# Optimization experiments

Measured on AMD Instinct MI355X. Metric: run time of the kernel, lower is better.

Reference implementation:

```python
import jax, jax.numpy as jnp
import numpy as np
import math

H = 5       # attention heads
DK = 20     # attdim // H
ATT = 100   # attdim
LAYERS = 2
B, L, BERT_DIM = 32, 256, 768


def _layernorm(x, a, b, eps=1e-6):
    mean = x.mean(-1, keepdims=True)
    std = jnp.std(x, axis=-1, ddof=1, keepdims=True)  # torch.std is unbiased
    return a * (x - mean) / (std + eps) + b


def _forward(sequence_output, src_mask, aspect_mask, short_mask,
             ln_a, ln_b, Wxx_w, Wxx_b, q_w, q_b, k_w, k_b,
             dense_w, dense_b, bias_m, W_w, W_b, Wx_w, Wx_b, clf_w, clf_b):
    Bn, Ln, _ = sequence_output.shape
    x = _layernorm(sequence_output, ln_a, ln_b)
    g = x @ Wxx_w + Wxx_b                                  # [B,L,100]
    asp_wn = aspect_mask.sum(1, keepdims=True)             # [B,1]
    aspect = (g * aspect_mask[..., None]).sum(1) / asp_wn  # [B,100]

    q = (g @ q_w + q_b).reshape(Bn, Ln, H, DK).transpose(0, 2, 1, 3)  # [B,H,L,dk]
    k = (g @ k_w + k_b).reshape(Bn, Ln, H, DK).transpose(0, 2, 1, 3)
    # aspect is expanded identically across heads/positions before dense -> [B,dk]
    asp = aspect @ dense_w + dense_b                       # [B,dk]
    scores = jnp.einsum('bhid,bhjd->bhij', q, k) / math.sqrt(DK)
    asp_sc = jnp.tanh(jnp.einsum('bd,bhjd->bhj', asp, k) + bias_m[0])
    scores = scores + asp_sc[:, :, None, :]
    scores = jnp.where(src_mask[:, None, None, :] == 0, -1e9, scores)
    scores = scores + short_mask                           # [B,1,L,L] broadcast
    adj = jax.nn.softmax(scores, axis=-1)                  # [B,H,L,L]

    # edge-update linear split so the [B,L,L,205] concat is never materialized:
    # edge[b,i,j] = adj_perm[b,i,j] @ Wa + go[b,j] @ W1 + go[b,i] @ W2 + b
    Wa, W1, W2 = Wx_w[:H], Wx_w[H:H + ATT], Wx_w[H + ATT:]
    go = g
    for i in range(LAYERS):
        # expand+matmul+mean over heads == mean-head message passing
        Ax = jnp.einsum('bhij,bjd->bid', adj, go) / H
        go = jax.nn.relu(Ax @ W_w + W_b)
        if i < LAYERS - 1:  # last edge update is discarded by the original output
            edge = (jnp.einsum('bhij,hk->bijk', adj, Wa)
                    + (go @ W1)[:, None, :, :]
                    + (go @ W2)[:, :, None, :]
                    + Wx_b)
            adj = edge.transpose(0, 3, 1, 2)
    # original: node_outputs = F.relu(gcn_outputs) (aggregate_W result is overwritten)
    h = jax.nn.relu(go)
    out1 = (h * aspect_mask[..., None]).sum(1) / asp_wn    # [B,100]
    return out1 @ clf_w + clf_b                            # [B,3]


def setup_inputs() -> dict:
    key = jax.random.key(0)
    ks = jax.random.split(key, 24)
    f32 = jnp.float32
    p = lambda k, shape, s=0.05: jax.random.normal(k, shape, dtype=f32) * s
    src_mask = jax.random.randint(ks[0], (B, L), 0, 2, dtype=jnp.int32).at[:, 0].set(1)
    aspect_mask = jnp.zeros((B, L), f32).at[:, 4:8].set(1.0)  # aspect span tokens
    return {
        'sequence_output': jax.random.normal(ks[1], (B, L, BERT_DIM), dtype=f32),
        'src_mask': src_mask,
        'aspect_mask': aspect_mask,
        'short_mask': p(ks[2], (B, 1, L, L), 1.0),
        'ln_a': jnp.ones((BERT_DIM,), f32),
        'ln_b': jnp.zeros((BERT_DIM,), f32),
        'Wxx_w': p(ks[3], (BERT_DIM, ATT)), 'Wxx_b': p(ks[4], (ATT,)),
        'q_w': p(ks[5], (ATT, ATT)), 'q_b': p(ks[6], (ATT,)),
        'k_w': p(ks[7], (ATT, ATT)), 'k_b': p(ks[8], (ATT,)),
        'dense_w': p(ks[9], (ATT, DK)), 'dense_b': p(ks[10], (DK,)),
        'bias_m': p(ks[11], (1,)),
        'W_w': p(ks[12], (ATT, ATT)), 'W_b': p(ks[13], (ATT,)),
        'Wx_w': p(ks[14], (H + 2 * ATT, H)), 'Wx_b': p(ks[15], (H,)),
        'clf_w': p(ks[16], (ATT, 3)), 'clf_b': p(ks[17], (3,)),
    }


def reference(sequence_output, src_mask, aspect_mask, short_mask,
              ln_a, ln_b, Wxx_w, Wxx_b, q_w, q_b, k_w, k_b,
              dense_w, dense_b, bias_m, W_w, W_b, Wx_w, Wx_b, clf_w, clf_b):
    return _forward(sequence_output, src_mask, aspect_mask, short_mask,
                    ln_a, ln_b, Wxx_w, Wxx_b, q_w, q_b, k_w, k_b,
                    dense_w, dense_b, bias_m, W_w, W_b, Wx_w, Wx_b, clf_w, clf_b)
```

## Files before the change

### kernel.cpp

```cpp
#include <hip/hip_runtime.h>
#include <math.h>

constexpr int CL = 256;
constexpr int CD = 768;
constexpr int CATT = 100;
constexpr int CH = 5;
constexpr int CDK = 20;

__device__ __forceinline__ void fma4(float4& a, float s, const float4& w) {
    a.x = fmaf(s, w.x, a.x);
    a.y = fmaf(s, w.y, a.y);
    a.z = fmaf(s, w.z, a.z);
    a.w = fmaf(s, w.w, a.w);
}

__global__ __launch_bounds__(256, 3) void k1_fused(
    const float* __restrict__ x, const float* __restrict__ ln_a,
    const float* __restrict__ ln_b, const float* __restrict__ Wxx_w,
    const float* __restrict__ Wxx_b, const float* __restrict__ q_w,
    const float* __restrict__ q_b, const float* __restrict__ k_w,
    const float* __restrict__ k_b, const float* __restrict__ amask,
    float* __restrict__ g, float* __restrict__ qt, float* __restrict__ ktb,
    float* __restrict__ aspect_raw)
{
    __shared__ float s_w[2][3200];
    __shared__ float s_xn[2][16 * 36];
    __shared__ float s_gt[16 * 100];
    __shared__ float s_ln[1536];
    __shared__ float s_mean[16], s_rinv[16];

    const int t = threadIdx.x;
    const int r0 = blockIdx.x * 16;
    const int wid = t >> 6, lane = t & 63;

    if (t < 192) {
        ((float4*)s_ln)[t] = ((const float4*)ln_a)[t];
        ((float4*)(s_ln + 768))[t] = ((const float4*)ln_b)[t];
    }

    for (int rr = wid * 4; rr < wid * 4 + 4; ++rr) {
        const float* xr = x + (size_t)(r0 + rr) * CD;
        float xv[12];
        float s = 0.f;
#pragma unroll
        for (int m = 0; m < 12; ++m) { xv[m] = xr[lane + 64 * m]; s += xv[m]; }
#pragma unroll
        for (int o = 32; o; o >>= 1) s += __shfl_xor(s, o);
        float mean = s * (1.0f / 768.0f);
        float sq = 0.f;
#pragma unroll
        for (int m = 0; m < 12; ++m) { float d = xv[m] - mean; sq = fmaf(d, d, sq); }
#pragma unroll
        for (int o = 32; o; o >>= 1) sq += __shfl_xor(sq, o);
        if (lane == 0) {
            s_mean[rr] = mean;
            s_rinv[rr] = 1.0f / (sqrtf(sq * (1.0f / 767.0f)) + 1e-6f);
        }
    }

    const float4* wsrc = (const float4*)Wxx_w;
    float4 w0 = wsrc[t], w1 = wsrc[t + 256], w2 = wsrc[t + 512], w3;
    if (t < 32) w3 = wsrc[t + 768];
    const int rA = t >> 5, cA = t & 31;
    float xa = x[(size_t)(r0 + rA) * CD + cA];
    float xb = x[(size_t)(r0 + rA + 8) * CD + cA];

    __syncthreads();

    {
        float4* d4 = (float4*)s_w[0];
        d4[t] = w0; d4[t + 256] = w1; d4[t + 512] = w2;
        if (t < 32) d4[t + 768] = w3;
        float la = s_ln[cA], lbv = s_ln[768 + cA];
        s_xn[0][rA * 36 + cA] = fmaf(la, (xa - s_mean[rA]) * s_rinv[rA], lbv);
        s_xn[0][(rA + 8) * 36 + cA] = fmaf(la, (xb - s_mean[rA + 8]) * s_rinv[rA + 8], lbv);
    }
    __syncthreads();

    const int cg = t % 25, rg = t / 25;
    const int c = cg * 4;
    float4 acc0 = make_float4(0.f, 0.f, 0.f, 0.f);
    float4 acc1 = make_float4(0.f, 0.f, 0.f, 0.f);

    for (int kt = 0; kt < 24; ++kt) {
        if (kt < 23) {
            const float4* ws = wsrc + (size_t)(kt + 1) * 800;
            w0 = ws[t]; w1 = ws[t + 256]; w2 = ws[t + 512];
            if (t < 32) w3 = ws[t + 768];
            int gc = (kt + 1) * 32 + cA;
            xa = x[(size_t)(r0 + rA) * CD + gc];
            xb = x[(size_t)(r0 + rA + 8) * CD + gc];
        }
        if (t < 200) {
            const float* wb = s_w[kt & 1];
            const float* xbuf = s_xn[kt & 1];
#pragma unroll 2
            for (int kk = 0; kk < 32; kk += 4) {
                float4 a0 = *(const float4*)&xbuf[(rg * 2 + 0) * 36 + kk];
                float4 a1 = *(const float4*)&xbuf[(rg * 2 + 1) * 36 + kk];
                float4 v0 = *(const float4*)&wb[(kk + 0) * 100 + c];
                float4 v1 = *(const float4*)&wb[(kk + 1) * 100 + c];
                float4 v2 = *(const float4*)&wb[(kk + 2) * 100 + c];
                float4 v3 = *(const float4*)&wb[(kk + 3) * 100 + c];
                fma4(acc0, a0.x, v0); fma4(acc0, a0.y, v1); fma4(acc0, a0.z, v2); fma4(acc0, a0.w, v3);
                fma4(acc1, a1.x, v0); fma4(acc1, a1.y, v1); fma4(acc1, a1.z, v2); fma4(acc1, a1.w, v3);
            }
        }
        if (kt < 23) {
            float4* d4 = (float4*)s_w[(kt + 1) & 1];
            d4[t] = w0; d4[t + 256] = w1; d4[t + 512] = w2;
            if (t < 32) d4[t + 768] = w3;
            int gc = (kt + 1) * 32 + cA;
            float la = s_ln[gc], lbv = s_ln[768 + gc];
            float* xd = s_xn[(kt + 1) & 1];
            xd[rA * 36 + cA] = fmaf(la, (xa - s_mean[rA]) * s_rinv[rA], lbv);
            xd[(rA + 8) * 36 + cA] = fmaf(la, (xb - s_mean[rA + 8]) * s_rinv[rA + 8], lbv);
        }
        __syncthreads();
    }

    if (t < 200) {
        float4 bias = *(const float4*)&Wxx_b[c];
        float4 rv0, rv1;
        rv0.x = acc0.x + bias.x; rv0.y = acc0.y + bias.y; rv0.z = acc0.z + bias.z; rv0.w = acc0.w + bias.w;
        rv1.x = acc1.x + bias.x; rv1.y = acc1.y + bias.y; rv1.z = acc1.z + bias.z; rv1.w = acc1.w + bias.w;
        float4 rv[2] = { rv0, rv1 };
#pragma unroll
        for (int q = 0; q < 2; ++q) {
            int row = r0 + rg * 2 + q;
            *(float4*)&g[(size_t)row * CATT + c] = rv[q];
            *(float4*)&s_gt[(rg * 2 + q) * 100 + c] = rv[q];
            float m = amask[row];
            if (m != 0.f) {
                int b = row >> 8;
                atomicAdd(&aspect_raw[b * CATT + c + 0], m * rv[q].x);
                atomicAdd(&aspect_raw[b * CATT + c + 1], m * rv[q].y);
                atomicAdd(&aspect_raw[b * CATT + c + 2], m * rv[q].z);
                atomicAdd(&aspect_raw[b * CATT + c + 3], m * rv[q].w);
            }
        }
    }

    const float4* qw4 = (const float4*)q_w;
    const float4* kw4 = (const float4*)k_w;
    float4 sA = qw4[t], sB;
    if (t < 244) sB = qw4[t + 256];
    __syncthreads();
    {
        float4* d4 = (float4*)s_w[0];
        d4[t] = sA; if (t < 244) d4[t + 256] = sB;
    }
    __syncthreads();

    float4 p0 = make_float4(0.f, 0.f, 0.f, 0.f);
    float4 p1 = make_float4(0.f, 0.f, 0.f, 0.f);
    for (int tau = 0; tau < 10; ++tau) {
        if (tau < 9) {
            const float4* src = (tau + 1 < 5) ? qw4 + (size_t)(tau + 1) * 500
                                              : kw4 + (size_t)(tau - 4) * 500;
            sA = src[t]; if (t < 244) sB = src[t + 256];
        }
        if (t < 200) {
            const float* wb = s_w[tau & 1];
            const int kb = (tau % 5) * 20;
#pragma unroll 2
            for (int kk = 0; kk < 20; kk += 4) {
                float4 a0 = *(const float4*)&s_gt[(rg * 2 + 0) * 100 + kb + kk];
                float4 a1 = *(const float4*)&s_gt[(rg * 2 + 1) * 100 + kb + kk];
                float4 v0 = *(const float4*)&wb[(kk + 0) * 100 + c];
                float4 v1 = *(const float4*)&wb[(kk + 1) * 100 + c];
                float4 v2 = *(const float4*)&wb[(kk + 2) * 100 + c];
                float4 v3 = *(const float4*)&wb[(kk + 3) * 100 + c];
                fma4(p0, a0.x, v0); fma4(p0, a0.y, v1); fma4(p0, a0.z, v2); fma4(p0, a0.w, v3);
                fma4(p1, a1.x, v0); fma4(p1, a1.y, v1); fma4(p1, a1.z, v2); fma4(p1, a1.w, v3);
            }
            if (tau == 4 || tau == 9) {
                const float* bb = (tau == 4) ? q_b : k_b;
                float* outp = (tau == 4) ? qt : ktb;
                float4 bias = *(const float4*)&bb[c];
                p0.x += bias.x; p0.y += bias.y; p0.z += bias.z; p0.w += bias.w;
                p1.x += bias.x; p1.y += bias.y; p1.z += bias.z; p1.w += bias.w;
                const int h = c / CDK, d = c % CDK;
                float4 rv[2] = { p0, p1 };
#pragma unroll
                for (int q = 0; q < 2; ++q) {
                    int row = r0 + rg * 2 + q;
                    int bidx = row >> 8, l = row & 255;
                    *(float4*)&outp[((size_t)(bidx * CH + h) * CL + l) * CDK + d] = rv[q];
                }
                p0 = make_float4(0.f, 0.f, 0.f, 0.f);
                p1 = make_float4(0.f, 0.f, 0.f, 0.f);
            }
        }
        if (tau < 9) {
            float4* d4 = (float4*)s_w[(tau + 1) & 1];
            d4[t] = sA; if (t < 244) d4[t + 256] = sB;
        }
        __syncthreads();
    }
}

__global__ __launch_bounds__(256, 3) void k45_attn_gcn0(
    const float* __restrict__ qt, const float* __restrict__ ktb,
    const float* __restrict__ aspect_raw, const float* __restrict__ amask,
    const float* __restrict__ dense_w, const float* __restrict__ dense_b,
    const float* __restrict__ bias_m, const int* __restrict__ src_mask,
    const float* __restrict__ shortm, const float* __restrict__ Wx_w,
    const float* __restrict__ g, const float* __restrict__ W_w,
    const float* __restrict__ W_b, float* __restrict__ adjW,
    float* __restrict__ go1, float* __restrict__ t1, float* __restrict__ t2,
    float* __restrict__ gW2S)
{
    constexpr int ICH = 16;
    __shared__ float s_pool[16 * 260];
    __shared__ float s_w[2][3200];
    __shared__ float s_q[CH * 320];
    __shared__ float s_red[CH][64];
    __shared__ float s_was[5];
    __shared__ float s_aspb[20];
    __shared__ float s_w1[100], s_w2[100];
    __shared__ float s_g1row[16];

    const int b = blockIdx.x >> 4, ic = blockIdx.x & 15;
    const int i0 = ic * ICH;
    const int t = threadIdx.x, lane = t & 63, wid = t >> 6;
    const int j = t;

    if (t < 5) {
        float s = 0.f;
        for (int k2 = 0; k2 < 5; ++k2) s += Wx_w[t * 5 + k2];
        s_was[t] = s;
    }
    if (t < 100) {
        float a = 0.f, c2 = 0.f;
#pragma unroll
        for (int h = 0; h < 5; ++h) {
            a += Wx_w[(5 + t) * 5 + h];
            c2 += Wx_w[(105 + t) * 5 + h];
        }
        s_w1[t] = a; s_w2[t] = c2;
    }
    float wn = 0.f;
    if (t < 64) {
        float4 mv = ((const float4*)amask)[b * 64 + t];
        wn = mv.x + mv.y + mv.z + mv.w;
#pragma unroll
        for (int o = 32; o; o >>= 1) wn += __shfl_xor(wn, o);
    }
    if (t < 20) {
        float a = 0.f;
        for (int d = 0; d < CATT; ++d)
            a = fmaf(aspect_raw[b * CATT + d], dense_w[d * CDK + t], a);
        s_aspb[t] = a / wn + dense_b[t];
    }
    {
        const float* qbase = qt + (size_t)b * CH * CL * CDK + (size_t)i0 * CDK;
        for (int i = t; i < CH * 320; i += 256) {
            int h = i / 320, r = i % 320;
            s_q[i] = qbase[(size_t)h * CL * CDK + r];
        }
    }

    const bool masked = (src_mask[b * CL + j] == 0);
    const float bm = bias_m[0];
    const float rs20 = 0.223606797749978969f;

    float sm[ICH];
#pragma unroll
    for (int ii = 0; ii < ICH; ++ii)
        sm[ii] = shortm[(size_t)(b * CL + i0 + ii) * CL + j];

    float accS[ICH], accW[ICH];
#pragma unroll
    for (int ii = 0; ii < ICH; ++ii) { accS[ii] = 0.f; accW[ii] = 0.f; }

    __syncthreads();

    for (int h = 0; h < CH; ++h) {
        float4 kr[5];
        const float* kp = ktb + ((size_t)(b * CH + h) * CL + j) * CDK;
#pragma unroll
        for (int m = 0; m < 5; ++m) kr[m] = *(const float4*)(kp + 4 * m);
        const float was_h = s_was[h];
        float s = bm;
#pragma unroll
        for (int m = 0; m < 5; ++m) {
            s = fmaf(s_aspb[4 * m + 0], kr[m].x, s);
            s = fmaf(s_aspb[4 * m + 1], kr[m].y, s);
            s = fmaf(s_aspb[4 * m + 2], kr[m].z, s);
            s = fmaf(s_aspb[4 * m + 3], kr[m].w, s);
        }
        const float aspsc = tanhf(s);

        float pv[ICH];
#pragma unroll
        for (int ii = 0; ii < ICH; ++ii) {
            const float* qrow = &s_q[h * 320 + ii * CDK];
            float sc = 0.f;
#pragma unroll
            for (int m = 0; m < 5; ++m) {
                float4 q4 = *(const float4*)(qrow + 4 * m);
                sc = fmaf(q4.x, kr[m].x, sc);
                sc = fmaf(q4.y, kr[m].y, sc);
                sc = fmaf(q4.z, kr[m].z, sc);
                sc = fmaf(q4.w, kr[m].w, sc);
            }
            sc = fmaf(sc, rs20, aspsc) + sm[ii];
            float p = masked ? 0.f : __expf(sc);
            pv[ii] = p;
            float ssum = p;
#pragma unroll
            for (int o = 32; o; o >>= 1) ssum += __shfl_xor(ssum, o);
            if (lane == 0) s_red[h][ii * 4 + wid] = ssum;
        }
        __syncthreads();
#pragma unroll
        for (int ii = 0; ii < ICH; ++ii) {
            float tot = s_red[h][ii * 4 + 0] + s_red[h][ii * 4 + 1] +
                        s_red[h][ii * 4 + 2] + s_red[h][ii * 4 + 3];
            float pn = pv[ii] * __frcp_rn(tot);
            accS[ii] += pn;
            accW[ii] = fmaf(was_h, pn, accW[ii]);
        }
    }

#pragma unroll
    for (int ii = 0; ii < ICH; ++ii) {
        adjW[(size_t)(b * CL + i0 + ii) * CL + j] = accW[ii];
        s_pool[ii * 260 + j] = accS[ii];
    }

    const int cg = t % 25, rg = t / 25;
    const int c = cg * 4;
    const float4* g4 = (const float4*)g + (size_t)b * 6400;
    float4 sA = g4[t], sB = g4[t + 256], sC = g4[t + 512], sD;
    if (t < 32) sD = g4[t + 768];
    {
        float4* d4 = (float4*)s_w[0];
        d4[t] = sA; d4[t + 256] = sB; d4[t + 512] = sC;
        if (t < 32) d4[t + 768] = sD;
    }
    __syncthreads();

    float4 acc0 = make_float4(0.f, 0.f, 0.f, 0.f);
    float4 acc1 = make_float4(0.f, 0.f, 0.f, 0.f);
    for (int jt = 0; jt < 8; ++jt) {
        if (jt < 7) {
            const float4* src = g4 + (size_t)(jt + 1) * 800;
            sA = src[t]; sB = src[t + 256]; sC = src[t + 512];
            if (t < 32) sD = src[t + 768];
        }
        if (t < 200) {
            const float* wb = s_w[jt & 1];
#pragma unroll 2
            for (int kk = 0; kk < 32; kk += 4) {
                float4 a0 = *(const float4*)&s_pool[(rg * 2 + 0) * 260 + jt * 32 + kk];
                float4 a1 = *(const float4*)&s_pool[(rg * 2 + 1) * 260 + jt * 32 + kk];
                float4 v0 = *(const float4*)&wb[(kk + 0) * 100 + c];
                float4 v1 = *(const float4*)&wb[(kk + 1) * 100 + c];
                float4 v2 = *(const float4*)&wb[(kk + 2) * 100 + c];
                float4 v3 = *(const float4*)&wb[(kk + 3) * 100 + c];
                fma4(acc0, a0.x, v0); fma4(acc0, a0.y, v1); fma4(acc0, a0.z, v2); fma4(acc0, a0.w, v3);
                fma4(acc1, a1.x, v0); fma4(acc1, a1.y, v1); fma4(acc1, a1.z, v2); fma4(acc1, a1.w, v3);
            }
        }
        if (jt < 7) {
            float4* d4 = (float4*)s_w[(jt + 1) & 1];
            d4[t] = sA; d4[t + 256] = sB; d4[t + 512] = sC;
            if (t < 32) d4[t + 768] = sD;
        }
        __syncthreads();
    }

    float* s_ax = s_pool;
    if (t < 200) {
        float4 r;
        r.x = acc0.x * 0.2f; r.y = acc0.y * 0.2f; r.z = acc0.z * 0.2f; r.w = acc0.w * 0.2f;
        *(float4*)&s_ax[(rg * 2 + 0) * 108 + c] = r;
        r.x = acc1.x * 0.2f; r.y = acc1.y * 0.2f; r.z = acc1.z * 0.2f; r.w = acc1.w * 0.2f;
        *(float4*)&s_ax[(rg * 2 + 1) * 108 + c] = r;
    }
    const float4* ww4 = (const float4*)W_w;
    sA = ww4[t]; if (t < 244) sB = ww4[t + 256];
    {
        float4* d4 = (float4*)s_w[0];
        d4[t] = sA; if (t < 244) d4[t + 256] = sB;
    }
    __syncthreads();

    float4 o0 = make_float4(0.f, 0.f, 0.f, 0.f);
    float4 o1 = make_float4(0.f, 0.f, 0.f, 0.f);
    for (int wt = 0; wt < 5; ++wt) {
        if (wt < 4) {
            const float4* src = ww4 + (size_t)(wt + 1) * 500;
            sA = src[t]; if (t < 244) sB = src[t + 256];
        }
        if (t < 200) {
            const float* wb = s_w[wt & 1];
            const int kb = wt * 20;
#pragma unroll 2
            for (int kk = 0; kk < 20; kk += 4) {
                float4 a0 = *(const float4*)&s_ax[(rg * 2 + 0) * 108 + kb + kk];
                float4 a1 = *(const float4*)&s_ax[(rg * 2 + 1) * 108 + kb + kk];
                float4 v0 = *(const float4*)&wb[(kk + 0) * 100 + c];
                float4 v1 = *(const float4*)&wb[(kk + 1) * 100 + c];
                float4 v2 = *(const float4*)&wb[(kk + 2) * 100 + c];
                float4 v3 = *(const float4*)&wb[(kk + 3) * 100 + c];
                fma4(o0, a0.x, v0); fma4(o0, a0.y, v1); fma4(o0, a0.z, v2); fma4(o0, a0.w, v3);
                fma4(o1, a1.x, v0); fma4(o1, a1.y, v1); fma4(o1, a1.z, v2); fma4(o1, a1.w, v3);
            }
        }
        if (wt < 4) {
            float4* d4 = (float4*)s_w[(wt + 1) & 1];
            d4[t] = sA; if (t < 244) d4[t + 256] = sB;
        }
        __syncthreads();
    }

    float* s_go = s_pool + 1728;
    if (t < 200) {
        float4 bias = *(const float4*)&W_b[c];
        o0.x = fmaxf(o0.x + bias.x, 0.f); o0.y = fmaxf(o0.y + bias.y, 0.f);
        o0.z = fmaxf(o0.z + bias.z, 0.f); o0.w = fmaxf(o0.w + bias.w, 0.f);
        o1.x = fmaxf(o1.x + bias.x, 0.f); o1.y = fmaxf(o1.y + bias.y, 0.f);
        o1.z = fmaxf(o1.z + bias.z, 0.f); o1.w = fmaxf(o1.w + bias.w, 0.f);
        *(float4*)&go1[(size_t)(b * CL + i0 + rg * 2 + 0) * CATT + c] = o0;
        *(float4*)&go1[(size_t)(b * CL + i0 + rg * 2 + 1) * CATT + c] = o1;
        *(float4*)&s_go[(rg * 2 + 0) * 104 + c] = o0;
        *(float4*)&s_go[(rg * 2 + 1) * 104 + c] = o1;
    }
    __syncthreads();

    if (t < 128) {
        int r = t >> 3, seg = t & 7;
        int e0 = seg * 13, e1 = e0 + 13 < 100 ? e0 + 13 : 100;
        float a = 0.f, c2 = 0.f;
        for (int e = e0; e < e1; ++e) {
            float v = s_go[r * 104 + e];
            a = fmaf(v, s_w1[e], a);
            c2 = fmaf(v, s_w2[e], c2);
        }
        a += __shfl_xor(a, 1); a += __shfl_xor(a, 2); a += __shfl_xor(a, 4);
        c2 += __shfl_xor(c2, 1); c2 += __shfl_xor(c2, 2); c2 += __shfl_xor(c2, 4);
        if (seg == 0) {
            s_g1row[r] = a;
            gW2S[b * CL + i0 + r] = c2;
        }
    }
    __syncthreads();

    if (t < 100) {
        float a = 0.f, s2 = 0.f;
#pragma unroll
        for (int r = 0; r < 16; ++r) {
            float v = s_go[r * 104 + t];
            a = fmaf(s_g1row[r], v, a);
            s2 += v;
        }
        atomicAdd(&t1[b * CATT + t], a);
        atomicAdd(&t2[b * CATT + t], s2);
    }
}

__global__ __launch_bounds__(256, 3) void k7_gcn1(
    const float* __restrict__ adjW, const float* __restrict__ go1,
    const float* __restrict__ W_w, const float* __restrict__ W_b,
    const float* __restrict__ t1, const float* __restrict__ t2,
    const float* __restrict__ gW2S, const float* __restrict__ Wx_b,
    const float* __restrict__ amask, float* __restrict__ out1_raw)
{
    __shared__ float s_pool[16 * 260];
    __shared__ float s_w[2][3200];
    const int b = blockIdx.x >> 4, ic = blockIdx.x & 15;
    const int i0 = ic * 16;
    const int t = threadIdx.x;

    {
        const float4* asrc = (const float4*)adjW + (size_t)(b * CL + i0) * 64;
#pragma unroll
        for (int m = 0; m < 4; ++m) {
            int i = t + 256 * m;
            int row = i >> 6, c4 = i & 63;
            *(float4*)&s_pool[row * 260 + c4 * 4] = asrc[i];
        }
    }
    const int cg = t % 25, rg = t / 25;
    const int c = cg * 4;
    const float4* g4 = (const float4*)go1 + (size_t)b * 6400;
    float4 sA = g4[t], sB = g4[t + 256], sC = g4[t + 512], sD;
    if (t < 32) sD = g4[t + 768];
    {
        float4* d4 = (float4*)s_w[0];
        d4[t] = sA; d4[t + 256] = sB; d4[t + 512] = sC;
        if (t < 32) d4[t + 768] = sD;
    }
    __syncthreads();

    float4 acc0 = make_float4(0.f, 0.f, 0.f, 0.f);
    float4 acc1 = make_float4(0.f, 0.f, 0.f, 0.f);
    for (int jt = 0; jt < 8; ++jt) {
        if (jt < 7) {
            const float4* src = g4 + (size_t)(jt + 1) * 800;
            sA = src[t]; sB = src[t + 256]; sC = src[t + 512];
            if (t < 32) sD = src[t + 768];
        }
        if (t < 200) {
            const float* wb = s_w[jt & 1];
#pragma unroll 2
            for (int kk = 0; kk < 32; kk += 4) {
                float4 a0 = *(const float4*)&s_pool[(rg * 2 + 0) * 260 + jt * 32 + kk];
                float4 a1 = *(const float4*)&s_pool[(rg * 2 + 1) * 260 + jt * 32 + kk];
                float4 v0 = *(const float4*)&wb[(kk + 0) * 100 + c];
                float4 v1 = *(const float4*)&wb[(kk + 1) * 100 + c];
                float4 v2 = *(const float4*)&wb[(kk + 2) * 100 + c];
                float4 v3 = *(const float4*)&wb[(kk + 3) * 100 + c];
                fma4(acc0, a0.x, v0); fma4(acc0, a0.y, v1); fma4(acc0, a0.z, v2); fma4(acc0, a0.w, v3);
                fma4(acc1, a1.x, v0); fma4(acc1, a1.y, v1); fma4(acc1, a1.z, v2); fma4(acc1, a1.w, v3);
            }
        }
        if (jt < 7) {
            float4* d4 = (float4*)s_w[(jt + 1) & 1];
            d4[t] = sA; d4[t + 256] = sB; d4[t + 512] = sC;
            if (t < 32) d4[t + 768] = sD;
        }
        __syncthreads();
    }

    float* s_ax = s_pool;
    if (t < 200) {
        float wxbs = Wx_b[0] + Wx_b[1] + Wx_b[2] + Wx_b[3] + Wx_b[4];
        float4 t1v = *(const float4*)&t1[b * CATT + c];
        float4 t2v = *(const float4*)&t2[b * CATT + c];
        float gw0 = gW2S[b * CL + i0 + rg * 2 + 0] + wxbs;
        float gw1 = gW2S[b * CL + i0 + rg * 2 + 1] + wxbs;
        float4 r;
        r.x = (acc0.x + t1v.x + gw0 * t2v.x) * 0.2f;
        r.y = (acc0.y + t1v.y + gw0 * t2v.y) * 0.2f;
        r.z = (acc0.z + t1v.z + gw0 * t2v.z) * 0.2f;
        r.w = (acc0.w + t1v.w + gw0 * t2v.w) * 0.2f;
        *(float4*)&s_ax[(rg * 2 + 0) * 108 + c] = r;
        r.x = (acc1.x + t1v.x + gw1 * t2v.x) * 0.2f;
        r.y = (acc1.y + t1v.y + gw1 * t2v.y) * 0.2f;
        r.z = (acc1.z + t1v.z + gw1 * t2v.z) * 0.2f;
        r.w = (acc1.w + t1v.w + gw1 * t2v.w) * 0.2f;
        *(float4*)&s_ax[(rg * 2 + 1) * 108 + c] = r;
    }
    const float4* ww4 = (const float4*)W_w;
    sA = ww4[t]; if (t < 244) sB = ww4[t + 256];
    {
        float4* d4 = (float4*)s_w[0];
        d4[t] = sA; if (t < 244) d4[t + 256] = sB;
    }
    __syncthreads();

    float4 o0 = make_float4(0.f, 0.f, 0.f, 0.f);
    float4 o1 = make_float4(0.f, 0.f, 0.f, 0.f);
    for (int wt = 0; wt < 5; ++wt) {
        if (wt < 4) {
            const float4* src = ww4 + (size_t)(wt + 1) * 500;
            sA = src[t]; if (t < 244) sB = src[t + 256];
        }
        if (t < 200) {
            const float* wb = s_w[wt & 1];
            const int kb = wt * 20;
#pragma unroll 2
            for (int kk = 0; kk < 20; kk += 4) {
                float4 a0 = *(const float4*)&s_ax[(rg * 2 + 0) * 108 + kb + kk];
                float4 a1 = *(const float4*)&s_ax[(rg * 2 + 1) * 108 + kb + kk];
                float4 v0 = *(const float4*)&wb[(kk + 0) * 100 + c];
                float4 v1 = *(const float4*)&wb[(kk + 1) * 100 + c];
                float4 v2 = *(const float4*)&wb[(kk + 2) * 100 + c];
                float4 v3 = *(const float4*)&wb[(kk + 3) * 100 + c];
                fma4(o0, a0.x, v0); fma4(o0, a0.y, v1); fma4(o0, a0.z, v2); fma4(o0, a0.w, v3);
                fma4(o1, a1.x, v0); fma4(o1, a1.y, v1); fma4(o1, a1.z, v2); fma4(o1, a1.w, v3);
            }
        }
        if (wt < 4) {
            float4* d4 = (float4*)s_w[(wt + 1) & 1];
            d4[t] = sA; if (t < 244) d4[t + 256] = sB;
        }
        __syncthreads();
    }

    if (t < 200) {
        float4 bias = *(const float4*)&W_b[c];
        o0.x = fmaxf(o0.x + bias.x, 0.f); o0.y = fmaxf(o0.y + bias.y, 0.f);
        o0.z = fmaxf(o0.z + bias.z, 0.f); o0.w = fmaxf(o0.w + bias.w, 0.f);
        o1.x = fmaxf(o1.x + bias.x, 0.f); o1.y = fmaxf(o1.y + bias.y, 0.f);
        o1.z = fmaxf(o1.z + bias.z, 0.f); o1.w = fmaxf(o1.w + bias.w, 0.f);
        float4 ov[2] = { o0, o1 };
#pragma unroll
        for (int q = 0; q < 2; ++q) {
            int row = b * CL + i0 + rg * 2 + q;
            float m = amask[row];
            if (m != 0.f) {
                atomicAdd(&out1_raw[b * CATT + c + 0], m * ov[q].x);
                atomicAdd(&out1_raw[b * CATT + c + 1], m * ov[q].y);
                atomicAdd(&out1_raw[b * CATT + c + 2], m * ov[q].z);
                atomicAdd(&out1_raw[b * CATT + c + 3], m * ov[q].w);
            }
        }
    }
}

__global__ __launch_bounds__(64) void k8_small(
    const float* __restrict__ out1_raw, const float* __restrict__ amask,
    const float* __restrict__ clf_w, const float* __restrict__ clf_b,
    float* __restrict__ out)
{
    const int b = blockIdx.x, t = threadIdx.x;
    float4 mv = ((const float4*)amask)[b * 64 + t];
    float wn = mv.x + mv.y + mv.z + mv.w;
#pragma unroll
    for (int o = 32; o; o >>= 1) wn += __shfl_xor(wn, o);
    if (t < 3) {
        float rwn = 1.f / wn;
        float a = clf_b[t];
        for (int d = 0; d < CATT; ++d)
            a = fmaf(out1_raw[b * CATT + d] * rwn, clf_w[d * 3 + t], a);
        out[b * 3 + t] = a;
    }
}

extern "C" void kernel_launch(void* const* d_in, const int* in_sizes, int n_in,
                              void* d_out, int out_size, void* d_ws, size_t ws_size,
                              hipStream_t stream) {
    const float* seq     = (const float*)d_in[0];
    const int*   srcm    = (const int*)d_in[1];
    const float* amask   = (const float*)d_in[2];
    const float* shortm  = (const float*)d_in[3];
    const float* ln_a    = (const float*)d_in[4];
    const float* ln_b    = (const float*)d_in[5];
    const float* Wxx_w   = (const float*)d_in[6];
    const float* Wxx_b   = (const float*)d_in[7];
    const float* q_w     = (const float*)d_in[8];
    const float* q_b     = (const float*)d_in[9];
    const float* k_w     = (const float*)d_in[10];
    const float* k_b     = (const float*)d_in[11];
    const float* dense_w = (const float*)d_in[12];
    const float* dense_b = (const float*)d_in[13];
    const float* bias_m  = (const float*)d_in[14];
    const float* W_w     = (const float*)d_in[15];
    const float* W_b     = (const float*)d_in[16];
    const float* Wx_w    = (const float*)d_in[17];
    const float* Wx_b    = (const float*)d_in[18];
    const float* clf_w   = (const float*)d_in[19];
    const float* clf_b   = (const float*)d_in[20];
    float* out = (float*)d_out;

    float* ws         = (float*)d_ws;
    float* g          = ws;
    float* qt         = g + 819200;
    float* ktb        = qt + 819200;
    float* go1        = ktb + 819200;
    float* adjW       = go1 + 819200;
    float* aspect_raw = adjW + 2097152;
    float* t1         = aspect_raw + 3200;
    float* t2         = t1 + 3200;
    float* out1_raw   = t2 + 3200;
    float* gW2S       = out1_raw + 3200;

    hipMemsetAsync(aspect_raw, 0, 4 * 3200 * sizeof(float), stream);
    hipLaunchKernelGGL(k1_fused, dim3(512), dim3(256), 0, stream, seq, ln_a, ln_b,
                       Wxx_w, Wxx_b, q_w, q_b, k_w, k_b, amask, g, qt, ktb, aspect_raw);
    hipLaunchKernelGGL(k45_attn_gcn0, dim3(512), dim3(256), 0, stream,
                       qt, ktb, aspect_raw, amask, dense_w, dense_b, bias_m, srcm,
                       shortm, Wx_w, g, W_w, W_b, adjW, go1, t1, t2, gW2S);
    hipLaunchKernelGGL(k7_gcn1, dim3(512), dim3(256), 0, stream,
                       adjW, go1, W_w, W_b, t1, t2, gW2S, Wx_b, amask, out1_raw);
    hipLaunchKernelGGL(k8_small, dim3(32), dim3(64), 0, stream,
                       out1_raw, amask, clf_w, clf_b, out);
}
```

Baseline: 242.9 us.

## Fuse all stages into one persistent kernel with atomic grid barriers

Replaces the four kernel launches with a single persistent kernel of 512 blocks that uses software grid-wide barriers (atomic counter plus spin-wait) between stages. The adjW intermediate buffer and the gW2S buffer are dropped, so the edge/adjacency data apparently stays in on-chip memory within a block across the GCN layers. This removes launch gaps and global round trips of intermediates. The cost is that all 512 blocks must be co-resident for the barrier not to deadlock (launch bounds 256,2), and the spin barrier adds its own latency.

```diff
diff --git a/kernel.cpp b/kernel.cpp
--- a/kernel.cpp
+++ b/kernel.cpp
@@ -6,6 +6,7 @@
 constexpr int CATT = 100;
 constexpr int CH = 5;
 constexpr int CDK = 20;
+constexpr unsigned NBLK = 512;
 
 __device__ __forceinline__ void fma4(float4& a, float s, const float4& w) {
     a.x = fmaf(s, w.x, a.x);
@@ -14,611 +15,621 @@
     a.w = fmaf(s, w.w, a.w);
 }
 
-__global__ __launch_bounds__(256, 3) void k1_fused(
-    const float* __restrict__ x, const float* __restrict__ ln_a,
-    const float* __restrict__ ln_b, const float* __restrict__ Wxx_w,
-    const float* __restrict__ Wxx_b, const float* __restrict__ q_w,
-    const float* __restrict__ q_b, const float* __restrict__ k_w,
-    const float* __restrict__ k_b, const float* __restrict__ amask,
-    float* __restrict__ g, float* __restrict__ qt, float* __restrict__ ktb,
-    float* __restrict__ aspect_raw)
-{
-    __shared__ float s_w[2][3200];
-    __shared__ float s_xn[2][16 * 36];
-    __shared__ float s_gt[16 * 100];
-    __shared__ float s_ln[1536];
-    __shared__ float s_mean[16], s_rinv[16];
-
-    const int t = threadIdx.x;
-    const int r0 = blockIdx.x * 16;
-    const int wid = t >> 6, lane = t & 63;
-
-    if (t < 192) {
-        ((float4*)s_ln)[t] = ((const float4*)ln_a)[t];
-        ((float4*)(s_ln + 768))[t] = ((const float4*)ln_b)[t];
-    }
-
-    for (int rr = wid * 4; rr < wid * 4 + 4; ++rr) {
-        const float* xr = x + (size_t)(r0 + rr) * CD;
-        float xv[12];
-        float s = 0.f;
-#pragma unroll
-        for (int m = 0; m < 12; ++m) { xv[m] = xr[lane + 64 * m]; s += xv[m]; }
-#pragma unroll
-        for (int o = 32; o; o >>= 1) s += __shfl_xor(s, o);
-        float mean = s * (1.0f / 768.0f);
-        float sq = 0.f;
-#pragma unroll
-        for (int m = 0; m < 12; ++m) { float d = xv[m] - mean; sq = fmaf(d, d, sq); }
-#pragma unroll
-        for (int o = 32; o; o >>= 1) sq += __shfl_xor(sq, o);
-        if (lane == 0) {
-            s_mean[rr] = mean;
-            s_rinv[rr] = 1.0f / (sqrtf(sq * (1.0f / 767.0f)) + 1e-6f);
-        }
-    }
-
-    const float4* wsrc = (const float4*)Wxx_w;
-    float4 w0 = wsrc[t], w1 = wsrc[t + 256], w2 = wsrc[t + 512], w3;
-    if (t < 32) w3 = wsrc[t + 768];
-    const int rA = t >> 5, cA = t & 31;
-    float xa = x[(size_t)(r0 + rA) * CD + cA];
-    float xb = x[(size_t)(r0 + rA + 8) * CD + cA];
-
+__device__ __forceinline__ void gbar(unsigned* bar, unsigned target) {
+    __threadfence();
     __syncthreads();
-
-    {
-        float4* d4 = (float4*)s_w[0];
-        d4[t] = w0; d4[t + 256] = w1; d4[t + 512] = w2;
-        if (t < 32) d4[t + 768] = w3;
-        float la = s_ln[cA], lbv = s_ln[768 + cA];
-        s_xn[0][rA * 36 + cA] = fmaf(la, (xa - s_mean[rA]) * s_rinv[rA], lbv);
-        s_xn[0][(rA + 8) * 36 + cA] = fmaf(la, (xb - s_mean[rA + 8]) * s_rinv[rA + 8], lbv);
+    if (threadIdx.x == 0) {
+        __hip_atomic_fetch_add(bar, 1u, __ATOMIC_RELEASE, __HIP_MEMORY_SCOPE_AGENT);
+        while (__hip_atomic_load(bar, __ATOMIC_ACQUIRE, __HIP_MEMORY_SCOPE_AGENT) < target) {
+            __builtin_amdgcn_s_sleep(8);
+        }
     }
     __syncthreads();
-
-    const int cg = t % 25, rg = t / 25;
-    const int c = cg * 4;
-    float4 acc0 = make_float4(0.f, 0.f, 0.f, 0.f);
-    float4 acc1 = make_float4(0.f, 0.f, 0.f, 0.f);
-
-    for (int kt = 0; kt < 24; ++kt) {
-        if (kt < 23) {
-            const float4* ws = wsrc + (size_t)(kt + 1) * 800;
-            w0 = ws[t]; w1 = ws[t + 256]; w2 = ws[t + 512];
-            if (t < 32) w3 = ws[t + 768];
-            int gc = (kt + 1) * 32 + cA;
-            xa = x[(size_t)(r0 + rA) * CD + gc];
-            xb = x[(size_t)(r0 + rA + 8) * CD + gc];
-        }
-        if (t < 200) {
-            const float* wb = s_w[kt & 1];
-            const float* xbuf = s_xn[kt & 1];
-#pragma unroll 2
-            for (int kk = 0; kk < 32; kk += 4) {
-                float4 a0 = *(const float4*)&xbuf[(rg * 2 + 0) * 36 + kk];
-                float4 a1 = *(const float4*)&xbuf[(rg * 2 + 1) * 36 + kk];
-                float4 v0 = *(const float4*)&wb[(kk + 0) * 100 + c];
-                float4 v1 = *(const float4*)&wb[(kk + 1) * 100 + c];
-                float4 v2 = *(const float4*)&wb[(kk + 2) * 100 + c];
-                float4 v3 = *(const float4*)&wb[(kk + 3) * 100 + c];
-                fma4(acc0, a0.x, v0); fma4(acc0, a0.y, v1); fma4(acc0, a0.z, v2); fma4(acc0, a0.w, v3);
-                fma4(acc1, a1.x, v0); fma4(acc1, a1.y, v1); fma4(acc1, a1.z, v2); fma4(acc1, a1.w, v3);
-            }
-        }
-        if (kt < 23) {
-            float4* d4 = (float4*)s_w[(kt + 1) & 1];
+    __threadfence();
+}
+
+__global__ __launch_bounds__(256, 2) void fused_all(
+    const float* __restrict__ x, const int* __restrict__ src_mask,
+    const float* __restrict__ amask, const float* __restrict__ shortm,
+    const float* __restrict__ ln_a, const float* __restrict__ ln_b,
+    const float* __restrict__ Wxx_w, const float* __restrict__ Wxx_b,
+    const float* __restrict__ q_w, const float* __restrict__ q_b,
+    const float* __restrict__ k_w, const float* __restrict__ k_b,
+    const float* __restrict__ dense_w, const float* __restrict__ dense_b,
+    const float* __restrict__ bias_m, const float* __restrict__ W_w,
+    const float* __restrict__ W_b, const float* __restrict__ Wx_w,
+    const float* __restrict__ Wx_b, const float* __restrict__ clf_w,
+    const float* __restrict__ clf_b,
+    float* __restrict__ g, float* __restrict__ qt, float* __restrict__ ktb,
+    float* __restrict__ go1, float* __restrict__ aspect_raw,
+    float* __restrict__ t1, float* __restrict__ t2,
+    float* __restrict__ out1_raw, unsigned* __restrict__ bar,
+    float* __restrict__ out)
+{
+    __shared__ __align__(16) float S[12744];
+
+    const int t = threadIdx.x;
+    const int lane = t & 63, wid = t >> 6;
+    const int blk = blockIdx.x;
+
+    {
+        float* s_wB   = S + 4160;
+        float* s_xn   = S + 0;
+        float* s_gt   = S + 1152;
+        float* s_ln   = S + 10560;
+        float* s_mean = S + 12160;
+        float* s_rinv = S + 12176;
+        const int r0 = blk * 16;
+
+        if (t < 192) {
+            ((float4*)s_ln)[t] = ((const float4*)ln_a)[t];
+            ((float4*)(s_ln + 768))[t] = ((const float4*)ln_b)[t];
+        }
+
+        for (int rr = wid * 4; rr < wid * 4 + 4; ++rr) {
+            const float* xr = x + (size_t)(r0 + rr) * CD;
+            float xv[12];
+            float s = 0.f;
+#pragma unroll
+            for (int m = 0; m < 12; ++m) { xv[m] = xr[lane + 64 * m]; s += xv[m]; }
+#pragma unroll
+            for (int o = 32; o; o >>= 1) s += __shfl_xor(s, o);
+            float mean = s * (1.0f / 768.0f);
+            float sq = 0.f;
+#pragma unroll
+            for (int m = 0; m < 12; ++m) { float d = xv[m] - mean; sq = fmaf(d, d, sq); }
+#pragma unroll
+            for (int o = 32; o; o >>= 1) sq += __shfl_xor(sq, o);
+            if (lane == 0) {
+                s_mean[rr] = mean;
+                s_rinv[rr] = 1.0f / (sqrtf(sq * (1.0f / 767.0f)) + 1e-6f);
+            }
+        }
+
+        const float4* wsrc = (const float4*)Wxx_w;
+        float4 w0 = wsrc[t], w1 = wsrc[t + 256], w2 = wsrc[t + 512], w3;
+        if (t < 32) w3 = wsrc[t + 768];
+        const int rA = t >> 5, cA = t & 31;
+        float xa = x[(size_t)(r0 + rA) * CD + cA];
+        float xb = x[(size_t)(r0 + rA + 8) * CD + cA];
+
+        __syncthreads();
+
+        {
+            float4* d4 = (float4*)s_wB;
             d4[t] = w0; d4[t + 256] = w1; d4[t + 512] = w2;
             if (t < 32) d4[t + 768] = w3;
-            int gc = (kt + 1) * 32 + cA;
-            float la = s_ln[gc], lbv = s_ln[768 + gc];
-            float* xd = s_xn[(kt + 1) & 1];
-            xd[rA * 36 + cA] = fmaf(la, (xa - s_mean[rA]) * s_rinv[rA], lbv);
-            xd[(rA + 8) * 36 + cA] = fmaf(la, (xb - s_mean[rA + 8]) * s_rinv[rA + 8], lbv);
-        }
-        __syncthreads();
+            float la = s_ln[cA], lbv = s_ln[768 + cA];
+            s_xn[rA * 36 + cA] = fmaf(la, (xa - s_mean[rA]) * s_rinv[rA], lbv);
+            s_xn[(rA + 8) * 36 + cA] = fmaf(la, (xb - s_mean[rA + 8]) * s_rinv[rA + 8], lbv);
+        }
+        __syncthreads();
+
+        const int cgi = t % 25, rg = t / 25;
+        const int c = cgi * 4;
+        float4 acc0 = make_float4(0.f, 0.f, 0.f, 0.f);
+        float4 acc1 = make_float4(0.f, 0.f, 0.f, 0.f);
+
+        for (int kt = 0; kt < 24; ++kt) {
+            if (kt < 23) {
+                const float4* ws = wsrc + (size_t)(kt + 1) * 800;
+                w0 = ws[t]; w1 = ws[t + 256]; w2 = ws[t + 512];
+                if (t < 32) w3 = ws[t + 768];
+                int gc = (kt + 1) * 32 + cA;
+                xa = x[(size_t)(r0 + rA) * CD + gc];
+                xb = x[(size_t)(r0 + rA + 8) * CD + gc];
+            }
+            if (t < 200) {
+                const float* wb = s_wB + (kt & 1) * 3200;
+                const float* xbuf = s_xn + (kt & 1) * 576;
+#pragma unroll 2
+                for (int kk = 0; kk < 32; kk += 4) {
+                    float4 a0 = *(const float4*)&xbuf[(rg * 2 + 0) * 36 + kk];
+                    float4 a1 = *(const float4*)&xbuf[(rg * 2 + 1) * 36 + kk];
+                    float4 v0 = *(const float4*)&wb[(kk + 0) * 100 + c];
+                    float4 v1 = *(const float4*)&wb[(kk + 1) * 100 + c];
+                    float4 v2 = *(const float4*)&wb[(kk + 2) * 100 + c];
+                    float4 v3 = *(const float4*)&wb[(kk + 3) * 100 + c];
+                    fma4(acc0, a0.x, v0); fma4(acc0, a0.y, v1); fma4(acc0, a0.z, v2); fma4(acc0, a0.w, v3);
+                    fma4(acc1, a1.x, v0); fma4(acc1, a1.y, v1); fma4(acc1, a1.z, v2); fma4(acc1, a1.w, v3);
+                }
+            }
+            if (kt < 23) {
+                float4* d4 = (float4*)(s_wB + ((kt + 1) & 1) * 3200);
+                d4[t] = w0; d4[t + 256] = w1; d4[t + 512] = w2;
+                if (t < 32) d4[t + 768] = w3;
+                int gc = (kt + 1) * 32 + cA;
+                float la = s_ln[gc], lbv = s_ln[768 + gc];
+                float* xd = s_xn + ((kt + 1) & 1) * 576;
+                xd[rA * 36 + cA] = fmaf(la, (xa - s_mean[rA]) * s_rinv[rA], lbv);
+                xd[(rA + 8) * 36 + cA] = fmaf(la, (xb - s_mean[rA + 8]) * s_rinv[rA + 8], lbv);
+            }
+            __syncthreads();
+        }
+
+        if (t < 200) {
+            float4 bias = *(const float4*)&Wxx_b[c];
+            float4 rv0, rv1;
+            rv0.x = acc0.x + bias.x; rv0.y = acc0.y + bias.y; rv0.z = acc0.z + bias.z; rv0.w = acc0.w + bias.w;
+            rv1.x = acc1.x + bias.x; rv1.y = acc1.y + bias.y; rv1.z = acc1.z + bias.z; rv1.w = acc1.w + bias.w;
+            float4 rv[2] = { rv0, rv1 };
+#pragma unroll
+            for (int q = 0; q < 2; ++q) {
+                int row = r0 + rg * 2 + q;
+                *(float4*)&g[(size_t)row * CATT + c] = rv[q];
+                *(float4*)&s_gt[(rg * 2 + q) * 100 + c] = rv[q];
+                float m = amask[row];
+                if (m != 0.f) {
+                    int b = row >> 8;
+                    atomicAdd(&aspect_raw[b * CATT + c + 0], m * rv[q].x);
+                    atomicAdd(&aspect_raw[b * CATT + c + 1], m * rv[q].y);
+                    atomicAdd(&aspect_raw[b * CATT + c + 2], m * rv[q].z);
+                    atomicAdd(&aspect_raw[b * CATT + c + 3], m * rv[q].w);
+                }
+            }
+        }
+
+        const float4* qw4 = (const float4*)q_w;
+        const float4* kw4 = (const float4*)k_w;
+        float4 sA = qw4[t], sB;
+        if (t < 244) sB = qw4[t + 256];
+        __syncthreads();
+        {
+            float4* d4 = (float4*)s_wB;
+            d4[t] = sA; if (t < 244) d4[t + 256] = sB;
+        }
+        __syncthreads();
+
+        float4 p0 = make_float4(0.f, 0.f, 0.f, 0.f);
+        float4 p1 = make_float4(0.f, 0.f, 0.f, 0.f);
+        for (int tau = 0; tau < 10; ++tau) {
+            if (tau < 9) {
+                const float4* src = (tau + 1 < 5) ? qw4 + (size_t)(tau + 1) * 500
+                                                  : kw4 + (size_t)(tau - 4) * 500;
+                sA = src[t]; if (t < 244) sB = src[t + 256];
+            }
+            if (t < 200) {
+                const float* wb = s_wB + (tau & 1) * 3200;
+                const int kb = (tau % 5) * 20;
+#pragma unroll 2
+                for (int kk = 0; kk < 20; kk += 4) {
+                    float4 a0 = *(const float4*)&s_gt[(rg * 2 + 0) * 100 + kb + kk];
+                    float4 a1 = *(const float4*)&s_gt[(rg * 2 + 1) * 100 + kb + kk];
+                    float4 v0 = *(const float4*)&wb[(kk + 0) * 100 + c];
+                    float4 v1 = *(const float4*)&wb[(kk + 1) * 100 + c];
+                    float4 v2 = *(const float4*)&wb[(kk + 2) * 100 + c];
+                    float4 v3 = *(const float4*)&wb[(kk + 3) * 100 + c];
+                    fma4(p0, a0.x, v0); fma4(p0, a0.y, v1); fma4(p0, a0.z, v2); fma4(p0, a0.w, v3);
+                    fma4(p1, a1.x, v0); fma4(p1, a1.y, v1); fma4(p1, a1.z, v2); fma4(p1, a1.w, v3);
+                }
+                if (tau == 4 || tau == 9) {
+                    const float* bb = (tau == 4) ? q_b : k_b;
+                    float* outp = (tau == 4) ? qt : ktb;
+                    float4 bias = *(const float4*)&bb[c];
+                    p0.x += bias.x; p0.y += bias.y; p0.z += bias.z; p0.w += bias.w;
+                    p1.x += bias.x; p1.y += bias.y; p1.z += bias.z; p1.w += bias.w;
+                    const int h = c / CDK, d = c % CDK;
+                    float4 rv[2] = { p0, p1 };
+#pragma unroll
+                    for (int q = 0; q < 2; ++q) {
+                        int row = r0 + rg * 2 + q;
+                        int bidx = row >> 8, l = row & 255;
+                        *(float4*)&outp[((size_t)(bidx * CH + h) * CL + l) * CDK + d] = rv[q];
+                    }
+                    p0 = make_float4(0.f, 0.f, 0.f, 0.f);
+                    p1 = make_float4(0.f, 0.f, 0.f, 0.f);
+                }
+            }
+            if (tau < 9) {
+                float4* d4 = (float4*)(s_wB + ((tau + 1) & 1) * 3200);
+                d4[t] = sA; if (t < 244) d4[t + 256] = sB;
+            }
+            __syncthreads();
+        }
     }
 
-    if (t < 200) {
-        float4 bias = *(const float4*)&Wxx_b[c];
-        float4 rv0, rv1;
-        rv0.x = acc0.x + bias.x; rv0.y = acc0.y + bias.y; rv0.z = acc0.z + bias.z; rv0.w = acc0.w + bias.w;
-        rv1.x = acc1.x + bias.x; rv1.y = acc1.y + bias.y; rv1.z = acc1.z + bias.z; rv1.w = acc1.w + bias.w;
-        float4 rv[2] = { rv0, rv1 };
-#pragma unroll
-        for (int q = 0; q < 2; ++q) {
-            int row = r0 + rg * 2 + q;
-            *(float4*)&g[(size_t)row * CATT + c] = rv[q];
-            *(float4*)&s_gt[(rg * 2 + q) * 100 + c] = rv[q];
-            float m = amask[row];
-            if (m != 0.f) {
-                int b = row >> 8;
-                atomicAdd(&aspect_raw[b * CATT + c + 0], m * rv[q].x);
-                atomicAdd(&aspect_raw[b * CATT + c + 1], m * rv[q].y);
-                atomicAdd(&aspect_raw[b * CATT + c + 2], m * rv[q].z);
-                atomicAdd(&aspect_raw[b * CATT + c + 3], m * rv[q].w);
-            }
-        }
-    }
-
-    const float4* qw4 = (const float4*)q_w;
-    const float4* kw4 = (const float4*)k_w;
-    float4 sA = qw4[t], sB;
-    if (t < 244) sB = qw4[t + 256];
-    __syncthreads();
+    gbar(bar, NBLK);
+
     {
-        float4* d4 = (float4*)s_w[0];
-        d4[t] = sA; if (t < 244) d4[t + 256] = sB;
-    }
-    __syncthreads();
-
-    float4 p0 = make_float4(0.f, 0.f, 0.f, 0.f);
-    float4 p1 = make_float4(0.f, 0.f, 0.f, 0.f);
-    for (int tau = 0; tau < 10; ++tau) {
-        if (tau < 9) {
-            const float4* src = (tau + 1 < 5) ? qw4 + (size_t)(tau + 1) * 500
-                                              : kw4 + (size_t)(tau - 4) * 500;
-            sA = src[t]; if (t < 244) sB = src[t + 256];
-        }
-        if (t < 200) {
-            const float* wb = s_w[tau & 1];
-            const int kb = (tau % 5) * 20;
-#pragma unroll 2
-            for (int kk = 0; kk < 20; kk += 4) {
-                float4 a0 = *(const float4*)&s_gt[(rg * 2 + 0) * 100 + kb + kk];
-                float4 a1 = *(const float4*)&s_gt[(rg * 2 + 1) * 100 + kb + kk];
-                float4 v0 = *(const float4*)&wb[(kk + 0) * 100 + c];
-                float4 v1 = *(const float4*)&wb[(kk + 1) * 100 + c];
-                float4 v2 = *(const float4*)&wb[(kk + 2) * 100 + c];
-                float4 v3 = *(const float4*)&wb[(kk + 3) * 100 + c];
-                fma4(p0, a0.x, v0); fma4(p0, a0.y, v1); fma4(p0, a0.z, v2); fma4(p0, a0.w, v3);
-                fma4(p1, a1.x, v0); fma4(p1, a1.y, v1); fma4(p1, a1.z, v2); fma4(p1, a1.w, v3);
-            }
-            if (tau == 4 || tau == 9) {
-                const float* bb = (tau == 4) ? q_b : k_b;
-                float* outp = (tau == 4) ? qt : ktb;
-                float4 bias = *(const float4*)&bb[c];
-                p0.x += bias.x; p0.y += bias.y; p0.z += bias.z; p0.w += bias.w;
-                p1.x += bias.x; p1.y += bias.y; p1.z += bias.z; p1.w += bias.w;
-                const int h = c / CDK, d = c % CDK;
-                float4 rv[2] = { p0, p1 };
-#pragma unroll
-                for (int q = 0; q < 2; ++q) {
-                    int row = r0 + rg * 2 + q;
-                    int bidx = row >> 8, l = row & 255;
-                    *(float4*)&outp[((size_t)(bidx * CH + h) * CL + l) * CDK + d] = rv[q];
-                }
-                p0 = make_float4(0.f, 0.f, 0.f, 0.f);
-                p1 = make_float4(0.f, 0.f, 0.f, 0.f);
-            }
-        }
-        if (tau < 9) {
-            float4* d4 = (float4*)s_w[(tau + 1) & 1];
-            d4[t] = sA; if (t < 244) d4[t + 256] = sB;
-        }
-        __syncthreads();
-    }
-}
-
-__global__ __launch_bounds__(256, 3) void k45_attn_gcn0(
-    const float* __restrict__ qt, const float* __restrict__ ktb,
-    const float* __restrict__ aspect_raw, const float* __restrict__ amask,
-    const float* __restrict__ dense_w, const float* __restrict__ dense_b,
-    const float* __restrict__ bias_m, const int* __restrict__ src_mask,
-    const float* __restrict__ shortm, const float* __restrict__ Wx_w,
-    const float* __restrict__ g, const float* __restrict__ W_w,
-    const float* __restrict__ W_b, float* __restrict__ adjW,
-    float* __restrict__ go1, float* __restrict__ t1, float* __restrict__ t2,
-    float* __restrict__ gW2S)
-{
-    constexpr int ICH = 16;
-    __shared__ float s_pool[16 * 260];
-    __shared__ float s_w[2][3200];
-    __shared__ float s_q[CH * 320];
-    __shared__ float s_red[CH][64];
-    __shared__ float s_was[5];
-    __shared__ float s_aspb[20];
-    __shared__ float s_w1[100], s_w2[100];
-    __shared__ float s_g1row[16];
-
-    const int b = blockIdx.x >> 4, ic = blockIdx.x & 15;
-    const int i0 = ic * ICH;
-    const int t = threadIdx.x, lane = t & 63, wid = t >> 6;
-    const int j = t;
-
-    if (t < 5) {
-        float s = 0.f;
-        for (int k2 = 0; k2 < 5; ++k2) s += Wx_w[t * 5 + k2];
-        s_was[t] = s;
-    }
-    if (t < 100) {
-        float a = 0.f, c2 = 0.f;
-#pragma unroll
-        for (int h = 0; h < 5; ++h) {
-            a += Wx_w[(5 + t) * 5 + h];
-            c2 += Wx_w[(105 + t) * 5 + h];
-        }
-        s_w1[t] = a; s_w2[t] = c2;
-    }
-    float wn = 0.f;
-    if (t < 64) {
-        float4 mv = ((const float4*)amask)[b * 64 + t];
-        wn = mv.x + mv.y + mv.z + mv.w;
-#pragma unroll
-        for (int o = 32; o; o >>= 1) wn += __shfl_xor(wn, o);
-    }
-    if (t < 20) {
-        float a = 0.f;
-        for (int d = 0; d < CATT; ++d)
-            a = fmaf(aspect_raw[b * CATT + d], dense_w[d * CDK + t], a);
-        s_aspb[t] = a / wn + dense_b[t];
-    }
-    {
-        const float* qbase = qt + (size_t)b * CH * CL * CDK + (size_t)i0 * CDK;
-        for (int i = t; i < CH * 320; i += 256) {
-            int h = i / 320, r = i % 320;
-            s_q[i] = qbase[(size_t)h * CL * CDK + r];
-        }
-    }
-
-    const bool masked = (src_mask[b * CL + j] == 0);
-    const float bm = bias_m[0];
-    const float rs20 = 0.223606797749978969f;
-
-    float sm[ICH];
-#pragma unroll
-    for (int ii = 0; ii < ICH; ++ii)
-        sm[ii] = shortm[(size_t)(b * CL + i0 + ii) * CL + j];
-
-    float accS[ICH], accW[ICH];
-#pragma unroll
-    for (int ii = 0; ii < ICH; ++ii) { accS[ii] = 0.f; accW[ii] = 0.f; }
-
-    __syncthreads();
-
-    for (int h = 0; h < CH; ++h) {
-        float4 kr[5];
-        const float* kp = ktb + ((size_t)(b * CH + h) * CL + j) * CDK;
-#pragma unroll
-        for (int m = 0; m < 5; ++m) kr[m] = *(const float4*)(kp + 4 * m);
-        const float was_h = s_was[h];
-        float s = bm;
-#pragma unroll
-        for (int m = 0; m < 5; ++m) {
-            s = fmaf(s_aspb[4 * m + 0], kr[m].x, s);
-            s = fmaf(s_aspb[4 * m + 1], kr[m].y, s);
-            s = fmaf(s_aspb[4 * m + 2], kr[m].z, s);
-            s = fmaf(s_aspb[4 * m + 3], kr[m].w, s);
-        }
-        const float aspsc = tanhf(s);
-
-        float pv[ICH];
-#pragma unroll
-        for (int ii = 0; ii < ICH; ++ii) {
-            const float* qrow = &s_q[h * 320 + ii * CDK];
-            float sc = 0.f;
+        constexpr int ICH = 16;
+        float* s_pool  = S + 0;
+        float* s_wB    = S + 4160;
+        float* s_q     = S + 10560;
+        float* s_red   = S + 12160;
+        float* s_was   = S + 12480;
+        float* s_aspb  = S + 12488;
+        float* s_w1    = S + 12512;
+        float* s_w2    = S + 12612;
+        float* s_g1row = S + 12712;
+        float* s_gw2   = S + 12728;
+
+        const int b = blk >> 4, ic = blk & 15;
+        const int i0 = ic * ICH;
+        const int j = t;
+
+        if (t < 5) {
+            float s = 0.f;
+            for (int k2 = 0; k2 < 5; ++k2) s += Wx_w[t * 5 + k2];
+            s_was[t] = s;
+        }
+        if (t < 100) {
+            float a = 0.f, c2 = 0.f;
+#pragma unroll
+            for (int h = 0; h < 5; ++h) {
+                a += Wx_w[(5 + t) * 5 + h];
+                c2 += Wx_w[(105 + t) * 5 + h];
+            }
+            s_w1[t] = a; s_w2[t] = c2;
+        }
+        float wn = 0.f;
+        if (t < 64) {
+            float4 mv = ((const float4*)amask)[b * 64 + t];
+            wn = mv.x + mv.y + mv.z + mv.w;
+#pragma unroll
+            for (int o = 32; o; o >>= 1) wn += __shfl_xor(wn, o);
+        }
+        if (t < 20) {
+            float a = 0.f;
+            for (int d = 0; d < CATT; ++d)
+                a = fmaf(aspect_raw[b * CATT + d], dense_w[d * CDK + t], a);
+            s_aspb[t] = a / wn + dense_b[t];
+        }
+        {
+            const float* qbase = qt + (size_t)b * CH * CL * CDK + (size_t)i0 * CDK;
+            for (int i = t; i < CH * 320; i += 256) {
+                int h = i / 320, r = i % 320;
+                s_q[i] = qbase[(size_t)h * CL * CDK + r];
+            }
+        }
+
+        const bool masked = (src_mask[b * CL + j] == 0);
+        const float bm = bias_m[0];
+        const float rs20 = 0.223606797749978969f;
+
+        float sm[ICH];
+#pragma unroll
+        for (int ii = 0; ii < ICH; ++ii)
+            sm[ii] = shortm[(size_t)(b * CL + i0 + ii) * CL + j];
+
+        float accS[ICH], accW[ICH];
+#pragma unroll
+        for (int ii = 0; ii < ICH; ++ii) { accS[ii] = 0.f; accW[ii] = 0.f; }
+
+        __syncthreads();
+
+        for (int h = 0; h < CH; ++h) {
+            float4 kr[5];
+            const float* kp = ktb + ((size_t)(b * CH + h) * CL + j) * CDK;
+#pragma unroll
+            for (int m = 0; m < 5; ++m) kr[m] = *(const float4*)(kp + 4 * m);
+            const float was_h = s_was[h];
+            float s = bm;
 #pragma unroll
             for (int m = 0; m < 5; ++m) {
-                float4 q4 = *(const float4*)(qrow + 4 * m);
-                sc = fmaf(q4.x, kr[m].x, sc);
-                sc = fmaf(q4.y, kr[m].y, sc);
-                sc = fmaf(q4.z, kr[m].z, sc);
-                sc = fmaf(q4.w, kr[m].w, sc);
-            }
-            sc = fmaf(sc, rs20, aspsc) + sm[ii];
-            float p = masked ? 0.f : __expf(sc);
-            pv[ii] = p;
-            float ssum = p;
-#pragma unroll
-            for (int o = 32; o; o >>= 1) ssum += __shfl_xor(ssum, o);
-            if (lane == 0) s_red[h][ii * 4 + wid] = ssum;
-        }
-        __syncthreads();
-#pragma unroll
-        for (int ii = 0; ii < ICH; ++ii) {
-            float tot = s_red[h][ii * 4 + 0] + s_red[h][ii * 4 + 1] +
-                        s_red[h][ii * 4 + 2] + s_red[h][ii * 4 + 3];
-            float pn = pv[ii] * __frcp_rn(tot);
-            accS[ii] += pn;
-            accW[ii] = fmaf(was_h, pn, accW[ii]);
-        }
-    }
-
-#pragma unroll
-    for (int ii = 0; ii < ICH; ++ii) {
-        adjW[(size_t)(b * CL + i0 + ii) * CL + j] = accW[ii];
-        s_pool[ii * 260 + j] = accS[ii];
-    }
-
-    const int cg = t % 25, rg = t / 25;
-    const int c = cg * 4;
-    const float4* g4 = (const float4*)g + (size_t)b * 6400;
-    float4 sA = g4[t], sB = g4[t + 256], sC = g4[t + 512], sD;
-    if (t < 32) sD = g4[t + 768];
-    {
-        float4* d4 = (float4*)s_w[0];
-        d4[t] = sA; d4[t + 256] = sB; d4[t + 512] = sC;
-        if (t < 32) d4[t + 768] = sD;
-    }
-    __syncthreads();
-
-    float4 acc0 = make_float4(0.f, 0.f, 0.f, 0.f);
-    float4 acc1 = make_float4(0.f, 0.f, 0.f, 0.f);
-    for (int jt = 0; jt < 8; ++jt) {
-        if (jt < 7) {
-            const float4* src = g4 + (size_t)(jt + 1) * 800;
-            sA = src[t]; sB = src[t + 256]; sC = src[t + 512];
-            if (t < 32) sD = src[t + 768];
-        }
-        if (t < 200) {
-            const float* wb = s_w[jt & 1];
-#pragma unroll 2
-            for (int kk = 0; kk < 32; kk += 4) {
-                float4 a0 = *(const float4*)&s_pool[(rg * 2 + 0) * 260 + jt * 32 + kk];
-                float4 a1 = *(const float4*)&s_pool[(rg * 2 + 1) * 260 + jt * 32 + kk];
-                float4 v0 = *(const float4*)&wb[(kk + 0) * 100 + c];
-                float4 v1 = *(const float4*)&wb[(kk + 1) * 100 + c];
-                float4 v2 = *(const float4*)&wb[(kk + 2) * 100 + c];
-                float4 v3 = *(const float4*)&wb[(kk + 3) * 100 + c];
-                fma4(acc0, a0.x, v0); fma4(acc0, a0.y, v1); fma4(acc0, a0.z, v2); fma4(acc0, a0.w, v3);
-                fma4(acc1, a1.x, v0); fma4(acc1, a1.y, v1); fma4(acc1, a1.z, v2); fma4(acc1, a1.w, v3);
-            }
-        }
-        if (jt < 7) {
-            float4* d4 = (float4*)s_w[(jt + 1) & 1];
+                s = fmaf(s_aspb[4 * m + 0], kr[m].x, s);
+                s = fmaf(s_aspb[4 * m + 1], kr[m].y, s);
+                s = fmaf(s_aspb[4 * m + 2], kr[m].z, s);
+                s = fmaf(s_aspb[4 * m + 3], kr[m].w, s);
+            }
+            const float aspsc = tanhf(s);
+
+            float pv[ICH];
+#pragma unroll
+            for (int ii = 0; ii < ICH; ++ii) {
+                const float* qrow = &s_q[h * 320 + ii * CDK];
+                float sc = 0.f;
+#pragma unroll
+                for (int m = 0; m < 5; ++m) {
+                    float4 q4 = *(const float4*)(qrow + 4 * m);
+                    sc = fmaf(q4.x, kr[m].x, sc);
+                    sc = fmaf(q4.y, kr[m].y, sc);
+                    sc = fmaf(q4.z, kr[m].z, sc);
+                    sc = fmaf(q4.w, kr[m].w, sc);
+                }
+                sc = fmaf(sc, rs20, aspsc) + sm[ii];
+                float p = masked ? 0.f : __expf(sc);
+                pv[ii] = p;
+                float ssum = p;
+#pragma unroll
+                for (int o = 32; o; o >>= 1) ssum += __shfl_xor(ssum, o);
+                if (lane == 0) s_red[h * 64 + ii * 4 + wid] = ssum;
+            }
+            __syncthreads();
+#pragma unroll
+            for (int ii = 0; ii < ICH; ++ii) {
+                float tot = s_red[h * 64 + ii * 4 + 0] + s_red[h * 64 + ii * 4 + 1] +
+                            s_red[h * 64 + ii * 4 + 2] + s_red[h * 64 + ii * 4 + 3];
+                float pn = pv[ii] * __frcp_rn(tot);
+                accS[ii] += pn;
+                accW[ii] = fmaf(was_h, pn, accW[ii]);
+            }
+        }
+
+#pragma unroll
+        for (int ii = 0; ii < ICH; ++ii)
+            s_pool[ii * 260 + j] = accS[ii];
+
+        const int cgi = t % 25, rg = t / 25;
+        const int c = cgi * 4;
+        const float4* g4 = (const float4*)g + (size_t)b * 6400;
+        float4 sA = g4[t], sB = g4[t + 256], sC = g4[t + 512], sD;
+        if (t < 32) sD = g4[t + 768];
+        {
+            float4* d4 = (float4*)s_wB;
             d4[t] = sA; d4[t + 256] = sB; d4[t + 512] = sC;
             if (t < 32) d4[t + 768] = sD;
         }
         __syncthreads();
+
+        float4 acc0 = make_float4(0.f, 0.f, 0.f, 0.f);
+        float4 acc1 = make_float4(0.f, 0.f, 0.f, 0.f);
+        for (int jt = 0; jt < 8; ++jt) {
+            if (jt < 7) {
+                const float4* src = g4 + (size_t)(jt + 1) * 800;
+                sA = src[t]; sB = src[t + 256]; sC = src[t + 512];
+                if (t < 32) sD = src[t + 768];
+            }
+            if (t < 200) {
+                const float* wb = s_wB + (jt & 1) * 3200;
+#pragma unroll 2
+                for (int kk = 0; kk < 32; kk += 4) {
+                    float4 a0 = *(const float4*)&s_pool[(rg * 2 + 0) * 260 + jt * 32 + kk];
+                    float4 a1 = *(const float4*)&s_pool[(rg * 2 + 1) * 260 + jt * 32 + kk];
+                    float4 v0 = *(const float4*)&wb[(kk + 0) * 100 + c];
+                    float4 v1 = *(const float4*)&wb[(kk + 1) * 100 + c];
+                    float4 v2 = *(const float4*)&wb[(kk + 2) * 100 + c];
+                    float4 v3 = *(const float4*)&wb[(kk + 3) * 100 + c];
+                    fma4(acc0, a0.x, v0); fma4(acc0, a0.y, v1); fma4(acc0, a0.z, v2); fma4(acc0, a0.w, v3);
+                    fma4(acc1, a1.x, v0); fma4(acc1, a1.y, v1); fma4(acc1, a1.z, v2); fma4(acc1, a1.w, v3);
+                }
+            }
+            if (jt < 7) {
+                float4* d4 = (float4*)(s_wB + ((jt + 1) & 1) * 3200);
+                d4[t] = sA; d4[t + 256] = sB; d4[t + 512] = sC;
+                if (t < 32) d4[t + 768] = sD;
+            }
+            __syncthreads();
+        }
+
+        float* s_ax = s_pool;
+        if (t < 200) {
+            float4 r;
+            r.x = acc0.x * 0.2f; r.y = acc0.y * 0.2f; r.z = acc0.z * 0.2f; r.w = acc0.w * 0.2f;
+            *(float4*)&s_ax[(rg * 2 + 0) * 108 + c] = r;
+            r.x = acc1.x * 0.2f; r.y = acc1.y * 0.2f; r.z = acc1.z * 0.2f; r.w = acc1.w * 0.2f;
+            *(float4*)&s_ax[(rg * 2 + 1) * 108 + c] = r;
+        }
+        const float4* ww4 = (const float4*)W_w;
+        sA = ww4[t]; if (t < 244) sB = ww4[t + 256];
+        {
+            float4* d4 = (float4*)s_wB;
+            d4[t] = sA; if (t < 244) d4[t + 256] = sB;
+        }
+        __syncthreads();
+
+        float4 o0 = make_float4(0.f, 0.f, 0.f, 0.f);
+        float4 o1 = make_float4(0.f, 0.f, 0.f, 0.f);
+        for (int wt = 0; wt < 5; ++wt) {
+            if (wt < 4) {
+                const float4* src = ww4 + (size_t)(wt + 1) * 500;
+                sA = src[t]; if (t < 244) sB = src[t + 256];
+            }
+            if (t < 200) {
+                const float* wb = s_wB + (wt & 1) * 3200;
+                const int kb = wt * 20;
+#pragma unroll 2
+                for (int kk = 0; kk < 20; kk += 4) {
+                    float4 a0 = *(const float4*)&s_ax[(rg * 2 + 0) * 108 + kb + kk];
+                    float4 a1 = *(const float4*)&s_ax[(rg * 2 + 1) * 108 + kb + kk];
+                    float4 v0 = *(const float4*)&wb[(kk + 0) * 100 + c];
+                    float4 v1 = *(const float4*)&wb[(kk + 1) * 100 + c];
+                    float4 v2 = *(const float4*)&wb[(kk + 2) * 100 + c];
+                    float4 v3 = *(const float4*)&wb[(kk + 3) * 100 + c];
+                    fma4(o0, a0.x, v0); fma4(o0, a0.y, v1); fma4(o0, a0.z, v2); fma4(o0, a0.w, v3);
+                    fma4(o1, a1.x, v0); fma4(o1, a1.y, v1); fma4(o1, a1.z, v2); fma4(o1, a1.w, v3);
+                }
+            }
+            if (wt < 4) {
+                float4* d4 = (float4*)(s_wB + ((wt + 1) & 1) * 3200);
+                d4[t] = sA; if (t < 244) d4[t + 256] = sB;
+            }
+            __syncthreads();
+        }
+
+        float* s_go = s_pool + 1728;
+        if (t < 200) {
+            float4 bias = *(const float4*)&W_b[c];
+            o0.x = fmaxf(o0.x + bias.x, 0.f); o0.y = fmaxf(o0.y + bias.y, 0.f);
+            o0.z = fmaxf(o0.z + bias.z, 0.f); o0.w = fmaxf(o0.w + bias.w, 0.f);
+            o1.x = fmaxf(o1.x + bias.x, 0.f); o1.y = fmaxf(o1.y + bias.y, 0.f);
+            o1.z = fmaxf(o1.z + bias.z, 0.f); o1.w = fmaxf(o1.w + bias.w, 0.f);
+            *(float4*)&go1[(size_t)(b * CL + i0 + rg * 2 + 0) * CATT + c] = o0;
+            *(float4*)&go1[(size_t)(b * CL + i0 + rg * 2 + 1) * CATT + c] = o1;
+            *(float4*)&s_go[(rg * 2 + 0) * 104 + c] = o0;
+            *(float4*)&s_go[(rg * 2 + 1) * 104 + c] = o1;
+        }
+        __syncthreads();
+
+        if (t < 128) {
+            int r = t >> 3, seg = t & 7;
+            int e0 = seg * 13, e1 = e0 + 13 < 100 ? e0 + 13 : 100;
+            float a = 0.f, c2 = 0.f;
+            for (int e = e0; e < e1; ++e) {
+                float v = s_go[r * 104 + e];
+                a = fmaf(v, s_w1[e], a);
+                c2 = fmaf(v, s_w2[e], c2);
+            }
+            a += __shfl_xor(a, 1); a += __shfl_xor(a, 2); a += __shfl_xor(a, 4);
+            c2 += __shfl_xor(c2, 1); c2 += __shfl_xor(c2, 2); c2 += __shfl_xor(c2, 4);
+            if (seg == 0) {
+                s_g1row[r] = a;
+                s_gw2[r] = c2;
+            }
+        }
+        __syncthreads();
+
+        if (t < 100) {
+            float a = 0.f, s2 = 0.f;
+#pragma unroll
+            for (int r = 0; r < 16; ++r) {
+                float v = s_go[r * 104 + t];
+                a = fmaf(s_g1row[r], v, a);
+                s2 += v;
+            }
+            atomicAdd(&t1[b * CATT + t], a);
+            atomicAdd(&t2[b * CATT + t], s2);
+        }
+        __syncthreads();
+
+#pragma unroll
+        for (int ii = 0; ii < ICH; ++ii)
+            s_pool[ii * 260 + j] = accW[ii];
     }
 
-    float* s_ax = s_pool;
-    if (t < 200) {
-        float4 r;
-        r.x = acc0.x * 0.2f; r.y = acc0.y * 0.2f; r.z = acc0.z * 0.2f; r.w = acc0.w * 0.2f;
-        *(float4*)&s_ax[(rg * 2 + 0) * 108 + c] = r;
-        r.x = acc1.x * 0.2f; r.y = acc1.y * 0.2f; r.z = acc1.z * 0.2f; r.w = acc1.w * 0.2f;
-        *(float4*)&s_ax[(rg * 2 + 1) * 108 + c] = r;
-    }
-    const float4* ww4 = (const float4*)W_w;
-    sA = ww4[t]; if (t < 244) sB = ww4[t + 256];
+    gbar(bar, 2 * NBLK);
+
     {
-        float4* d4 = (float4*)s_w[0];
-        d4[t] = sA; if (t < 244) d4[t + 256] = sB;
-    }
-    __syncthreads();
-
-    float4 o0 = make_float4(0.f, 0.f, 0.f, 0.f);
-    float4 o1 = make_float4(0.f, 0.f, 0.f, 0.f);
-    for (int wt = 0; wt < 5; ++wt) {
-        if (wt < 4) {
-            const float4* src = ww4 + (size_t)(wt + 1) * 500;
-            sA = src[t]; if (t < 244) sB = src[t + 256];
-        }
-        if (t < 200) {
-            const float* wb = s_w[wt & 1];
-            const int kb = wt * 20;
-#pragma unroll 2
-            for (int kk = 0; kk < 20; kk += 4) {
-                float4 a0 = *(const float4*)&s_ax[(rg * 2 + 0) * 108 + kb + kk];
-                float4 a1 = *(const float4*)&s_ax[(rg * 2 + 1) * 108 + kb + kk];
-                float4 v0 = *(const float4*)&wb[(kk + 0) * 100 + c];
-                float4 v1 = *(const float4*)&wb[(kk + 1) * 100 + c];
-                float4 v2 = *(const float4*)&wb[(kk + 2) * 100 + c];
-                float4 v3 = *(const float4*)&wb[(kk + 3) * 100 + c];
-                fma4(o0, a0.x, v0); fma4(o0, a0.y, v1); fma4(o0, a0.z, v2); fma4(o0, a0.w, v3);
-                fma4(o1, a1.x, v0); fma4(o1, a1.y, v1); fma4(o1, a1.z, v2); fma4(o1, a1.w, v3);
-            }
-        }
-        if (wt < 4) {
-            float4* d4 = (float4*)s_w[(wt + 1) & 1];
-            d4[t] = sA; if (t < 244) d4[t + 256] = sB;
-        }
-        __syncthreads();
-    }
-
-    float* s_go = s_pool + 1728;
-    if (t < 200) {
-        float4 bias = *(const float4*)&W_b[c];
-        o0.x = fmaxf(o0.x + bias.x, 0.f); o0.y = fmaxf(o0.y + bias.y, 0.f);
-        o0.z = fmaxf(o0.z + bias.z, 0.f); o0.w = fmaxf(o0.w + bias.w, 0.f);
-        o1.x = fmaxf(o1.x + bias.x, 0.f); o1.y = fmaxf(o1.y + bias.y, 0.f);
-        o1.z = fmaxf(o1.z + bias.z, 0.f); o1.w = fmaxf(o1.w + bias.w, 0.f);
-        *(float4*)&go1[(size_t)(b * CL + i0 + rg * 2 + 0) * CATT + c] = o0;
-        *(float4*)&go1[(size_t)(b * CL + i0 + rg * 2 + 1) * CATT + c] = o1;
-        *(float4*)&s_go[(rg * 2 + 0) * 104 + c] = o0;
-        *(float4*)&s_go[(rg * 2 + 1) * 104 + c] = o1;
-    }
-    __syncthreads();
-
-    if (t < 128) {
-        int r = t >> 3, seg = t & 7;
-        int e0 = seg * 13, e1 = e0 + 13 < 100 ? e0 + 13 : 100;
-        float a = 0.f, c2 = 0.f;
-        for (int e = e0; e < e1; ++e) {
-            float v = s_go[r * 104 + e];
-            a = fmaf(v, s_w1[e], a);
-            c2 = fmaf(v, s_w2[e], c2);
-        }
-        a += __shfl_xor(a, 1); a += __shfl_xor(a, 2); a += __shfl_xor(a, 4);
-        c2 += __shfl_xor(c2, 1); c2 += __shfl_xor(c2, 2); c2 += __shfl_xor(c2, 4);
-        if (seg == 0) {
-            s_g1row[r] = a;
-            gW2S[b * CL + i0 + r] = c2;
-        }
-    }
-    __syncthreads();
-
-    if (t < 100) {
-        float a = 0.f, s2 = 0.f;
-#pragma unroll
-        for (int r = 0; r < 16; ++r) {
-            float v = s_go[r * 104 + t];
-            a = fmaf(s_g1row[r], v, a);
-            s2 += v;
-        }
-        atomicAdd(&t1[b * CATT + t], a);
-        atomicAdd(&t2[b * CATT + t], s2);
-    }
-}
-
-__global__ __launch_bounds__(256, 3) void k7_gcn1(
-    const float* __restrict__ adjW, const float* __restrict__ go1,
-    const float* __restrict__ W_w, const float* __restrict__ W_b,
-    const float* __restrict__ t1, const float* __restrict__ t2,
-    const float* __restrict__ gW2S, const float* __restrict__ Wx_b,
-    const float* __restrict__ amask, float* __restrict__ out1_raw)
-{
-    __shared__ float s_pool[16 * 260];
-    __shared__ float s_w[2][3200];
-    const int b = blockIdx.x >> 4, ic = blockIdx.x & 15;
-    const int i0 = ic * 16;
-    const int t = threadIdx.x;
-
-    {
-        const float4* asrc = (const float4*)adjW + (size_t)(b * CL + i0) * 64;
-#pragma unroll
-        for (int m = 0; m < 4; ++m) {
-            int i = t + 256 * m;
-            int row = i >> 6, c4 = i & 63;
-            *(float4*)&s_pool[row * 260 + c4 * 4] = asrc[i];
-        }
-    }
-    const int cg = t % 25, rg = t / 25;
-    const int c = cg * 4;
-    const float4* g4 = (const float4*)go1 + (size_t)b * 6400;
-    float4 sA = g4[t], sB = g4[t + 256], sC = g4[t + 512], sD;
-    if (t < 32) sD = g4[t + 768];
-    {
-        float4* d4 = (float4*)s_w[0];
-        d4[t] = sA; d4[t + 256] = sB; d4[t + 512] = sC;
-        if (t < 32) d4[t + 768] = sD;
-    }
-    __syncthreads();
-
-    float4 acc0 = make_float4(0.f, 0.f, 0.f, 0.f);
-    float4 acc1 = make_float4(0.f, 0.f, 0.f, 0.f);
-    for (int jt = 0; jt < 8; ++jt) {
-        if (jt < 7) {
-            const float4* src = g4 + (size_t)(jt + 1) * 800;
-            sA = src[t]; sB = src[t + 256]; sC = src[t + 512];
-            if (t < 32) sD = src[t + 768];
-        }
-        if (t < 200) {
-            const float* wb = s_w[jt & 1];
-#pragma unroll 2
-            for (int kk = 0; kk < 32; kk += 4) {
-                float4 a0 = *(const float4*)&s_pool[(rg * 2 + 0) * 260 + jt * 32 + kk];
-                float4 a1 = *(const float4*)&s_pool[(rg * 2 + 1) * 260 + jt * 32 + kk];
-                float4 v0 = *(const float4*)&wb[(kk + 0) * 100 + c];
-                float4 v1 = *(const float4*)&wb[(kk + 1) * 100 + c];
-                float4 v2 = *(const float4*)&wb[(kk + 2) * 100 + c];
-                float4 v3 = *(const float4*)&wb[(kk + 3) * 100 + c];
-                fma4(acc0, a0.x, v0); fma4(acc0, a0.y, v1); fma4(acc0, a0.z, v2); fma4(acc0, a0.w, v3);
-                fma4(acc1, a1.x, v0); fma4(acc1, a1.y, v1); fma4(acc1, a1.z, v2); fma4(acc1, a1.w, v3);
-            }
-        }
-        if (jt < 7) {
-            float4* d4 = (float4*)s_w[(jt + 1) & 1];
+        float* s_pool = S + 0;
+        float* s_wB   = S + 4160;
+        float* s_gw2  = S + 12728;
+
+        const int b = blk >> 4, ic = blk & 15;
+        const int i0 = ic * 16;
+        const int cgi = t % 25, rg = t / 25;
+        const int c = cgi * 4;
+
+        const float4* g4 = (const float4*)go1 + (size_t)b * 6400;
+        float4 sA = g4[t], sB = g4[t + 256], sC = g4[t + 512], sD;
+        if (t < 32) sD = g4[t + 768];
+        {
+            float4* d4 = (float4*)s_wB;
             d4[t] = sA; d4[t + 256] = sB; d4[t + 512] = sC;
             if (t < 32) d4[t + 768] = sD;
         }
         __syncthreads();
+
+        float4 acc0 = make_float4(0.f, 0.f, 0.f, 0.f);
+        float4 acc1 = make_float4(0.f, 0.f, 0.f, 0.f);
+        for (int jt = 0; jt < 8; ++jt) {
+            if (jt < 7) {
+                const float4* src = g4 + (size_t)(jt + 1) * 800;
+                sA = src[t]; sB = src[t + 256]; sC = src[t + 512];
+                if (t < 32) sD = src[t + 768];
+            }
+            if (t < 200) {
+                const float* wb = s_wB + (jt & 1) * 3200;
+#pragma unroll 2
+                for (int kk = 0; kk < 32; kk += 4) {
+                    float4 a0 = *(const float4*)&s_pool[(rg * 2 + 0) * 260 + jt * 32 + kk];
+                    float4 a1 = *(const float4*)&s_pool[(rg * 2 + 1) * 260 + jt * 32 + kk];
+                    float4 v0 = *(const float4*)&wb[(kk + 0) * 100 + c];
+                    float4 v1 = *(const float4*)&wb[(kk + 1) * 100 + c];
+                    float4 v2 = *(const float4*)&wb[(kk + 2) * 100 + c];
+                    float4 v3 = *(const float4*)&wb[(kk + 3) * 100 + c];
+                    fma4(acc0, a0.x, v0); fma4(acc0, a0.y, v1); fma4(acc0, a0.z, v2); fma4(acc0, a0.w, v3);
+                    fma4(acc1, a1.x, v0); fma4(acc1, a1.y, v1); fma4(acc1, a1.z, v2); fma4(acc1, a1.w, v3);
+                }
+            }
+            if (jt < 7) {
+                float4* d4 = (float4*)(s_wB + ((jt + 1) & 1) * 3200);
+                d4[t] = sA; d4[t + 256] = sB; d4[t + 512] = sC;
+                if (t < 32) d4[t + 768] = sD;
+            }
+            __syncthreads();
+        }
+
+        float* s_ax = s_pool;
+        if (t < 200) {
+            float wxbs = Wx_b[0] + Wx_b[1] + Wx_b[2] + Wx_b[3] + Wx_b[4];
+            float4 t1v = *(const float4*)&t1[b * CATT + c];
+            float4 t2v = *(const float4*)&t2[b * CATT + c];
+            float gw0 = s_gw2[rg * 2 + 0] + wxbs;
+            float gw1 = s_gw2[rg * 2 + 1] + wxbs;
+            float4 r;
+            r.x = (acc0.x + t1v.x + gw0 * t2v.x) * 0.2f;
+            r.y = (acc0.y + t1v.y + gw0 * t2v.y) * 0.2f;
+            r.z = (acc0.z + t1v.z + gw0 * t2v.z) * 0.2f;
+            r.w = (acc0.w + t1v.w + gw0 * t2v.w) * 0.2f;
+            *(float4*)&s_ax[(rg * 2 + 0) * 108 + c] = r;
+            r.x = (acc1.x + t1v.x + gw1 * t2v.x) * 0.2f;
+            r.y = (acc1.y + t1v.y + gw1 * t2v.y) * 0.2f;
+            r.z = (acc1.z + t1v.z + gw1 * t2v.z) * 0.2f;
+            r.w = (acc1.w + t1v.w + gw1 * t2v.w) * 0.2f;
+            *(float4*)&s_ax[(rg * 2 + 1) * 108 + c] = r;
+        }
+        const float4* ww4 = (const float4*)W_w;
+        sA = ww4[t]; if (t < 244) sB = ww4[t + 256];
+        {
+            float4* d4 = (float4*)s_wB;
+            d4[t] = sA; if (t < 244) d4[t + 256] = sB;
+        }
+        __syncthreads();
+
+        float4 o0 = make_float4(0.f, 0.f, 0.f, 0.f);
+        float4 o1 = make_float4(0.f, 0.f, 0.f, 0.f);
+        for (int wt = 0; wt < 5; ++wt) {
+            if (wt < 4) {
+                const float4* src = ww4 + (size_t)(wt + 1) * 500;
+                sA = src[t]; if (t < 244) sB = src[t + 256];
+            }
+            if (t < 200) {
+                const float* wb = s_wB + (wt & 1) * 3200;
+                const int kb = wt * 20;
+#pragma unroll 2
+                for (int kk = 0; kk < 20; kk += 4) {
+                    float4 a0 = *(const float4*)&s_ax[(rg * 2 + 0) * 108 + kb + kk];
+                    float4 a1 = *(const float4*)&s_ax[(rg * 2 + 1) * 108 + kb + kk];
+                    float4 v0 = *(const float4*)&wb[(kk + 0) * 100 + c];
+                    float4 v1 = *(const float4*)&wb[(kk + 1) * 100 + c];
+                    float4 v2 = *(const float4*)&wb[(kk + 2) * 100 + c];
+                    float4 v3 = *(const float4*)&wb[(kk + 3) * 100 + c];
+                    fma4(o0, a0.x, v0); fma4(o0, a0.y, v1); fma4(o0, a0.z, v2); fma4(o0, a0.w, v3);
+                    fma4(o1, a1.x, v0); fma4(o1, a1.y, v1); fma4(o1, a1.z, v2); fma4(o1, a1.w, v3);
+                }
+            }
+            if (wt < 4) {
+                float4* d4 = (float4*)(s_wB + ((wt + 1) & 1) * 3200);
+                d4[t] = sA; if (t < 244) d4[t + 256] = sB;
+            }
+            __syncthreads();
+        }
+
+        if (t < 200) {
+            float4 bias = *(const float4*)&W_b[c];
+            o0.x = fmaxf(o0.x + bias.x, 0.f); o0.y = fmaxf(o0.y + bias.y, 0.f);
+            o0.z = fmaxf(o0.z + bias.z, 0.f); o0.w = fmaxf(o0.w + bias.w, 0.f);
+            o1.x = fmaxf(o1.x + bias.x, 0.f); o1.y = fmaxf(o1.y + bias.y, 0.f);
+            o1.z = fmaxf(o1.z + bias.z, 0.f); o1.w = fmaxf(o1.w + bias.w, 0.f);
+            float4 ov[2] = { o0, o1 };
+#pragma unroll
+            for (int q = 0; q < 2; ++q) {
+                int row = b * CL + i0 + rg * 2 + q;
+                float m = amask[row];
+                if (m != 0.f) {
+                    atomicAdd(&out1_raw[b * CATT + c + 0], m * ov[q].x);
+                    atomicAdd(&out1_raw[b * CATT + c + 1], m * ov[q].y);
+                    atomicAdd(&out1_raw[b * CATT + c + 2], m * ov[q].z);
+                    atomicAdd(&out1_raw[b * CATT + c + 3], m * ov[q].w);
+                }
+            }
+        }
     }
 
-    float* s_ax = s_pool;
-    if (t < 200) {
-        float wxbs = Wx_b[0] + Wx_b[1] + Wx_b[2] + Wx_b[3] + Wx_b[4];
-        float4 t1v = *(const float4*)&t1[b * CATT + c];
-        float4 t2v = *(const float4*)&t2[b * CATT + c];
-        float gw0 = gW2S[b * CL + i0 + rg * 2 + 0] + wxbs;
-        float gw1 = gW2S[b * CL + i0 + rg * 2 + 1] + wxbs;
-        float4 r;
-        r.x = (acc0.x + t1v.x + gw0 * t2v.x) * 0.2f;
-        r.y = (acc0.y + t1v.y + gw0 * t2v.y) * 0.2f;
-        r.z = (acc0.z + t1v.z + gw0 * t2v.z) * 0.2f;
-        r.w = (acc0.w + t1v.w + gw0 * t2v.w) * 0.2f;
-        *(float4*)&s_ax[(rg * 2 + 0) * 108 + c] = r;
-        r.x = (acc1.x + t1v.x + gw1 * t2v.x) * 0.2f;
-        r.y = (acc1.y + t1v.y + gw1 * t2v.y) * 0.2f;
-        r.z = (acc1.z + t1v.z + gw1 * t2v.z) * 0.2f;
-        r.w = (acc1.w + t1v.w + gw1 * t2v.w) * 0.2f;
-        *(float4*)&s_ax[(rg * 2 + 1) * 108 + c] = r;
-    }
-    const float4* ww4 = (const float4*)W_w;
-    sA = ww4[t]; if (t < 244) sB = ww4[t + 256];
-    {
-        float4* d4 = (float4*)s_w[0];
-        d4[t] = sA; if (t < 244) d4[t + 256] = sB;
-    }
-    __syncthreads();
-
-    float4 o0 = make_float4(0.f, 0.f, 0.f, 0.f);
-    float4 o1 = make_float4(0.f, 0.f, 0.f, 0.f);
-    for (int wt = 0; wt < 5; ++wt) {
-        if (wt < 4) {
-            const float4* src = ww4 + (size_t)(wt + 1) * 500;
-            sA = src[t]; if (t < 244) sB = src[t + 256];
-        }
-        if (t < 200) {
-            const float* wb = s_w[wt & 1];
-            const int kb = wt * 20;
-#pragma unroll 2
-            for (int kk = 0; kk < 20; kk += 4) {
-                float4 a0 = *(const float4*)&s_ax[(rg * 2 + 0) * 108 + kb + kk];
-                float4 a1 = *(const float4*)&s_ax[(rg * 2 + 1) * 108 + kb + kk];
-                float4 v0 = *(const float4*)&wb[(kk + 0) * 100 + c];
-                float4 v1 = *(const float4*)&wb[(kk + 1) * 100 + c];
-                float4 v2 = *(const float4*)&wb[(kk + 2) * 100 + c];
-                float4 v3 = *(const float4*)&wb[(kk + 3) * 100 + c];
-                fma4(o0, a0.x, v0); fma4(o0, a0.y, v1); fma4(o0, a0.z, v2); fma4(o0, a0.w, v3);
-                fma4(o1, a1.x, v0); fma4(o1, a1.y, v1); fma4(o1, a1.z, v2); fma4(o1, a1.w, v3);
-            }
-        }
-        if (wt < 4) {
-            float4* d4 = (float4*)s_w[(wt + 1) & 1];
-            d4[t] = sA; if (t < 244) d4[t + 256] = sB;
-        }
-        __syncthreads();
-    }
-
-    if (t < 200) {
-        float4 bias = *(const float4*)&W_b[c];
-        o0.x = fmaxf(o0.x + bias.x, 0.f); o0.y = fmaxf(o0.y + bias.y, 0.f);
-        o0.z = fmaxf(o0.z + bias.z, 0.f); o0.w = fmaxf(o0.w + bias.w, 0.f);
-        o1.x = fmaxf(o1.x + bias.x, 0.f); o1.y = fmaxf(o1.y + bias.y, 0.f);
-        o1.z = fmaxf(o1.z + bias.z, 0.f); o1.w = fmaxf(o1.w + bias.w, 0.f);
-        float4 ov[2] = { o0, o1 };
-#pragma unroll
-        for (int q = 0; q < 2; ++q) {
-            int row = b * CL + i0 + rg * 2 + q;
-            float m = amask[row];
-            if (m != 0.f) {
-                atomicAdd(&out1_raw[b * CATT + c + 0], m * ov[q].x);
-                atomicAdd(&out1_raw[b * CATT + c + 1], m * ov[q].y);
-                atomicAdd(&out1_raw[b * CATT + c + 2], m * ov[q].z);
-                atomicAdd(&out1_raw[b * CATT + c + 3], m * ov[q].w);
-            }
-        }
-    }
-}
-
-__global__ __launch_bounds__(64) void k8_small(
-    const float* __restrict__ out1_raw, const float* __restrict__ amask,
-    const float* __restrict__ clf_w, const float* __restrict__ clf_b,
-    float* __restrict__ out)
-{
-    const int b = blockIdx.x, t = threadIdx.x;
-    float4 mv = ((const float4*)amask)[b * 64 + t];
-    float wn = mv.x + mv.y + mv.z + mv.w;
-#pragma unroll
-    for (int o = 32; o; o >>= 1) wn += __shfl_xor(wn, o);
-    if (t < 3) {
-        float rwn = 1.f / wn;
-        float a = clf_b[t];
-        for (int d = 0; d < CATT; ++d)
-            a = fmaf(out1_raw[b * CATT + d] * rwn, clf_w[d * 3 + t], a);
-        out[b * 3 + t] = a;
+    gbar(bar, 3 * NBLK);
+
+    if (blk < 32 && t < 64) {
+        const int b = blk;
+        float4 mv = ((const float4*)amask)[b * 64 + t];
+        float wn = mv.x + mv.y + mv.z + mv.w;
+#pragma unroll
+        for (int o = 32; o; o >>= 1) wn += __shfl_xor(wn, o);
+        if (t < 3) {
+            float rwn = 1.f / wn;
+            float a = clf_b[t];
+            for (int d = 0; d < CATT; ++d)
+                a = fmaf(out1_raw[b * CATT + d] * rwn, clf_w[d * 3 + t], a);
+            out[b * 3 + t] = a;
+        }
     }
 }
 
@@ -653,21 +664,17 @@
     float* qt         = g + 819200;
     float* ktb        = qt + 819200;
     float* go1        = ktb + 819200;
-    float* adjW       = go1 + 819200;
-    float* aspect_raw = adjW + 2097152;
+    float* aspect_raw = go1 + 819200;
     float* t1         = aspect_raw + 3200;
     float* t2         = t1 + 3200;
     float* out1_raw   = t2 + 3200;
-    float* gW2S       = out1_raw + 3200;
-
-    hipMemsetAsync(aspect_raw, 0, 4 * 3200 * sizeof(float), stream);
-    hipLaunchKernelGGL(k1_fused, dim3(512), dim3(256), 0, stream, seq, ln_a, ln_b,
-                       Wxx_w, Wxx_b, q_w, q_b, k_w, k_b, amask, g, qt, ktb, aspect_raw);
-    hipLaunchKernelGGL(k45_attn_gcn0, dim3(512), dim3(256), 0, stream,
-                       qt, ktb, aspect_raw, amask, dense_w, dense_b, bias_m, srcm,
-                       shortm, Wx_w, g, W_w, W_b, adjW, go1, t1, t2, gW2S);
-    hipLaunchKernelGGL(k7_gcn1, dim3(512), dim3(256), 0, stream,
-                       adjW, go1, W_w, W_b, t1, t2, gW2S, Wx_b, amask, out1_raw);
-    hipLaunchKernelGGL(k8_small, dim3(32), dim3(64), 0, stream,
-                       out1_raw, amask, clf_w, clf_b, out);
+    unsigned* bar     = (unsigned*)(out1_raw + 3200);
+
+    hipMemsetAsync(aspect_raw, 0, (4 * 3200 + 16) * sizeof(float), stream);
+
+    hipLaunchKernelGGL(fused_all, dim3(NBLK), dim3(256), 0, stream,
+                       seq, srcm, amask, shortm, ln_a, ln_b, Wxx_w, Wxx_b,
+                       q_w, q_b, k_w, k_b, dense_w, dense_b, bias_m,
+                       W_w, W_b, Wx_w, Wx_b, clf_w, clf_b,
+                       g, qt, ktb, go1, aspect_raw, t1, t2, out1_raw, bar, out);
 }
```

Result: slower. 583.5 us (+140.3%).
